# Kernel tuning notes

Measured on AMD Instinct MI355X. Metric: run time of the kernel, lower is better.

The kernel has to match this reference:

```python
import jax, jax.numpy as jnp
import numpy as np

# ---- dims (see shape_source) ----
N, EG, T = 10000, 120000, 600000
NR, NS = 16, 7                      # num_radial, num_spherical
EA, EE, ET, ERBF, ECBF, EBIL = 128, 256, 64, 16, 16, 64
NB = 2                              # num_blocks
CUTOFF = 6.0
MAXZ = 100
INV_SQRT2 = 0.7071067811865476


def scaled_silu(x):
    # GemNet 'swish' activation = ScaledSiLU
    return jax.nn.silu(x) * (1.0 / 0.6)


def layer_norm(x, w, b):
    mu = jnp.mean(x, -1, keepdims=True)
    v = jnp.var(x, -1, keepdims=True)
    return (x - mu) * jax.lax.rsqrt(v + 1e-5) * w + b


def radial_basis(D):
    # polynomial envelope (exponent 5) * gaussian RBF on d/cutoff
    d = D / CUTOFF
    p = 5.0
    env = 1.0 - ((p + 1) * (p + 2) / 2) * d**5 + p * (p + 2) * d**6 - (p * (p + 1) / 2) * d**7
    env = jnp.where(d < 1.0, env, 0.0)
    offsets = jnp.linspace(0.0, 1.0, NR)
    coeff = -0.5 * (NR - 1.0) ** 2   # -0.5 / spacing^2
    return env[:, None] * jnp.exp(coeff * (d[:, None] - offsets) ** 2)  # (EG, NR)


def spherical_basis(cosphi):
    # circular basis: Y_l0(phi) = sqrt((2l+1)/4pi) P_l(cos phi), l = 0..NS-1
    P = [jnp.ones_like(cosphi), cosphi]
    for l in range(2, NS):
        P.append(((2 * l - 1) * cosphi * P[-1] - (l - 1) * P[-2]) / l)
    return jnp.stack([np.sqrt((2 * l + 1) / (4 * np.pi)) * P[l] for l in range(NS)], -1)  # (T, NS)


def residual(x, Ws):
    # GemNet ResidualLayer: 2 bias-free dense + skip, scaled by 1/sqrt(2)
    y = scaled_silu(scaled_silu(x @ Ws[0]) @ Ws[1])
    return (x + y) * INV_SQRT2


def gemnet_forward(D, cosphi, atom_emb, W_rbf3, W_rbf_h, W_rbf_out, W_cbf_down,
                   W_edge_emb, ib_dense_ca, ib_trip_dense_ba, ib_trip_mlp_rbf,
                   ib_trip_down, ib_trip_bilinear, ib_trip_up_ca, ib_trip_up_ac,
                   ib_res_before, ib_res_after, ib_atom_dense_rbf, ib_atom_dense1,
                   ib_atom_res, ib_concat_dense, ib_res_m, ob_dense_rbf, ob_dense1,
                   ob_res, ln_m_w, ln_m_b, ln_E_w, ln_E_b,
                   Z, idx_s, idx_t, id3_ba, id3_ca, id_swap):
    rbf = radial_basis(D)                                   # (EG, NR)
    sph = spherical_basis(cosphi)                           # (T, NS)
    rbf3 = rbf @ W_rbf3                                     # (EG, ERBF)
    rbf_h = rbf @ W_rbf_h
    rbf_out = rbf @ W_rbf_out
    # EfficientInteractionDownProjection: rbf x W -> (EG, NS, ECBF)
    rbf_W1 = jnp.einsum('er,sri->esi', rbf, W_cbf_down)
    # per-triplet circular-basis embedding: sum over spherical components
    cbf_t = jnp.einsum('ts,tsi->ti', sph, rbf_W1[id3_ca])   # (T, ECBF)

    h = atom_emb[Z]                                         # (N, EA)
    m = scaled_silu(jnp.concatenate([h[idx_s], h[idx_t], rbf], -1) @ W_edge_emb)  # (EG, EE)

    def out_block(i, h_cur, m_cur):
        mn = layer_norm(m_cur, ln_m_w[i], ln_m_b[i])
        x = mn * (rbf_out @ ob_dense_rbf[i])                # (EG, EE)
        xE = jax.ops.segment_sum(x, idx_t, num_segments=N)  # scatter edges -> atoms
        xE = scaled_silu(xE @ ob_dense1[i])                 # (N, EA)
        for r in range(ob_res.shape[1]):
            xE = residual(xE, ob_res[i, r])
        return layer_norm(xE, ln_E_w[i], ln_E_b[i])

    E_t = out_block(0, h, m)
    for i in range(NB):
        # ---- triplet interaction ----
        x_ca_skip = scaled_silu(m @ ib_dense_ca[i])
        x_ba = scaled_silu(m @ ib_trip_dense_ba[i])
        x_ba = x_ba * (rbf3 @ ib_trip_mlp_rbf[i])
        x_trip = scaled_silu(x_ba @ ib_trip_down[i])        # (EG, ET)
        x_t = x_trip[id3_ba]                                # gather -> (T, ET)
        # bilinear: out[t,o] = sum_i cbf_t[t,i] * sum_c x_t[t,c] W[c,i,o]
        Wb = ib_trip_bilinear[i]                            # (ET, ECBF, EBIL)
        acc = (x_t @ Wb[:, 0, :]) * cbf_t[:, 0:1]
        for ic in range(1, ECBF):
            acc = acc + (x_t @ Wb[:, ic, :]) * cbf_t[:, ic:ic + 1]
        x = jax.ops.segment_sum(acc, id3_ca, num_segments=EG)  # scatter trip -> edges (EG, EBIL)
        x_ca = scaled_silu(x @ ib_trip_up_ca[i])
        x_ac = scaled_silu(x @ ib_trip_up_ac[i])[id_swap]   # counter-directional edge
        x3 = (x_ca + x_ac) * INV_SQRT2

        # ---- edge update ----
        x = (x_ca_skip + x3) * INV_SQRT2
        for r in range(ib_res_before.shape[1]):
            x = residual(x, ib_res_before[i, r])
        x = (x + m) * INV_SQRT2
        for r in range(ib_res_after.shape[1]):
            x = residual(x, ib_res_after[i, r])

        # ---- atom update ----
        xa = x * (rbf_h @ ib_atom_dense_rbf[i])
        xa = jax.ops.segment_sum(xa, idx_t, num_segments=N)
        xa = scaled_silu(xa @ ib_atom_dense1[i])            # (N, EA)
        for r in range(ib_atom_res.shape[1]):
            xa = residual(xa, ib_atom_res[i, r])
        h = (h + xa) * INV_SQRT2

        # ---- edge embedding refresh with updated atoms ----
        m2 = scaled_silu(jnp.concatenate([h[idx_s], h[idx_t], x], -1) @ ib_concat_dense[i])
        for r in range(ib_res_m.shape[1]):
            m2 = residual(m2, ib_res_m[i, r])
        m = (m + m2) * INV_SQRT2

        E_t = E_t + out_block(i + 1, h, m)
    return E_t  # (N, EA) per-atom output features


def setup_inputs() -> dict:
    key = jax.random.key(0)
    ks = iter(jax.random.split(key, 64))

    def nrm(shape, fan_in):
        return jax.random.normal(next(ks), shape, jnp.float32) / np.sqrt(fan_in)

    Z = jax.random.randint(next(ks), (N,), 0, MAXZ)
    idx_s = jax.random.randint(next(ks), (EG,), 0, N)
    idx_t = jax.random.randint(next(ks), (EG,), 0, N)
    id3_ba = jax.random.randint(next(ks), (T,), 0, EG)
    id3_ca = jax.random.randint(next(ks), (T,), 0, EG)
    id_swap = jnp.arange(EG) ^ 1   # symmetric edges stored in (e, e^1) pairs
    D = jax.random.uniform(next(ks), (EG,), jnp.float32, 0.8, 5.9)
    cosphi = jax.random.uniform(next(ks), (T,), jnp.float32, -1.0, 1.0)

    emb = jax.random.normal(next(ks), (MAXZ, EA), jnp.float32)
    emb = emb / jnp.maximum(jnp.linalg.norm(emb, axis=-1, keepdims=True), 1.0)  # max_norm=1

    NBo = NB + 1
    inp = dict(
        D=D, cosphi=cosphi, atom_emb=emb,
        W_rbf3=nrm((NR, ERBF), NR), W_rbf_h=nrm((NR, ERBF), NR), W_rbf_out=nrm((NR, ERBF), NR),
        W_cbf_down=nrm((NS, NR, ECBF), NR),
        W_edge_emb=nrm((2 * EA + NR, EE), 2 * EA + NR),
        ib_dense_ca=nrm((NB, EE, EE), EE),
        ib_trip_dense_ba=nrm((NB, EE, EE), EE),
        ib_trip_mlp_rbf=nrm((NB, ERBF, EE), ERBF),
        ib_trip_down=nrm((NB, EE, ET), EE),
        ib_trip_bilinear=nrm((NB, ET, ECBF, EBIL), ET * ECBF),
        ib_trip_up_ca=nrm((NB, EBIL, EE), EBIL),
        ib_trip_up_ac=nrm((NB, EBIL, EE), EBIL),
        ib_res_before=nrm((NB, 1, 2, EE, EE), EE),
        ib_res_after=nrm((NB, 1, 2, EE, EE), EE),
        ib_atom_dense_rbf=nrm((NB, ERBF, EE), ERBF),
        ib_atom_dense1=nrm((NB, EE, EA), EE),
        ib_atom_res=nrm((NB, 2, 2, EA, EA), EA),
        ib_concat_dense=nrm((NB, 2 * EA + EE, EE), 2 * EA + EE),
        ib_res_m=nrm((NB, 1, 2, EE, EE), EE),
        ob_dense_rbf=nrm((NBo, ERBF, EE), ERBF),
        ob_dense1=nrm((NBo, EE, EA), EE),
        ob_res=nrm((NBo, 2, 2, EA, EA), EA),
        ln_m_w=jnp.ones((NBo, EE)), ln_m_b=jnp.zeros((NBo, EE)),
        ln_E_w=jnp.ones((NBo, EA)), ln_E_b=jnp.zeros((NBo, EA)),
        Z=Z, idx_s=idx_s, idx_t=idx_t, id3_ba=id3_ba, id3_ca=id3_ca, id_swap=id_swap,
    )
    return inp


def reference(D, cosphi, atom_emb, W_rbf3, W_rbf_h, W_rbf_out, W_cbf_down, W_edge_emb,
              ib_dense_ca, ib_trip_dense_ba, ib_trip_mlp_rbf, ib_trip_down,
              ib_trip_bilinear, ib_trip_up_ca, ib_trip_up_ac, ib_res_before,
              ib_res_after, ib_atom_dense_rbf, ib_atom_dense1, ib_atom_res,
              ib_concat_dense, ib_res_m, ob_dense_rbf, ob_dense1, ob_res,
              ln_m_w, ln_m_b, ln_E_w, ln_E_b, Z, idx_s, idx_t, id3_ba, id3_ca, id_swap):
    return gemnet_forward(D, cosphi, atom_emb, W_rbf3, W_rbf_h, W_rbf_out, W_cbf_down,
                          W_edge_emb, ib_dense_ca, ib_trip_dense_ba, ib_trip_mlp_rbf,
                          ib_trip_down, ib_trip_bilinear, ib_trip_up_ca, ib_trip_up_ac,
                          ib_res_before, ib_res_after, ib_atom_dense_rbf, ib_atom_dense1,
                          ib_atom_res, ib_concat_dense, ib_res_m, ob_dense_rbf, ob_dense1,
                          ob_res, ln_m_w, ln_m_b, ln_E_w, ln_E_b,
                          Z, idx_s, idx_t, id3_ba, id3_ca, id_swap)
```

## Files before the change

kernel.cpp:

```cpp
#include <hip/hip_runtime.h>

#define NATOM 10000
#define EG    120000
#define TT    600000

#define INV_SQRT2f 0.7071067811865476f

typedef unsigned short bf16t;
typedef __attribute__((ext_vector_type(8))) short s16x8;
typedef __attribute__((ext_vector_type(8))) unsigned short u16x8;
typedef __attribute__((ext_vector_type(4))) float f32x4;

__device__ __forceinline__ float ssilu(float x) {
    return x * (1.0f / (1.0f + __expf(-x))) * (1.0f / 0.6f);
}
__device__ __forceinline__ float bf2f(unsigned short u) {
    return __uint_as_float(((unsigned)u) << 16);
}
__device__ __forceinline__ unsigned short f2bf(float f) {
    unsigned b = __float_as_uint(f);
    unsigned r = (b + 0x7FFF + ((b >> 16) & 1)) >> 16;
    return (unsigned short)r;
}
__device__ __forceinline__ u16x8 cvt8(const float4 va, const float4 vb) {
    u16x8 r{};
    r[0] = f2bf(va.x); r[1] = f2bf(va.y); r[2] = f2bf(va.z); r[3] = f2bf(va.w);
    r[4] = f2bf(vb.x); r[5] = f2bf(vb.y); r[6] = f2bf(vb.z); r[7] = f2bf(vb.w);
    return r;
}

template <typename T> struct VT;
template <> struct VT<float> {
    static __device__ __forceinline__ float4 load4(const float* p) { return *(const float4*)p; }
    static __device__ __forceinline__ void store4(float* p, float4 v) { *(float4*)p = v; }
    static __device__ __forceinline__ float load(const float* p) { return *p; }
    static __device__ __forceinline__ void store(float* p, float v) { *p = v; }
};
template <> struct VT<bf16t> {
    static __device__ __forceinline__ float4 load4(const bf16t* p) {
        ushort4 u = *(const ushort4*)p;
        return make_float4(bf2f(u.x), bf2f(u.y), bf2f(u.z), bf2f(u.w));
    }
    static __device__ __forceinline__ void store4(bf16t* p, float4 v) {
        ushort4 u; u.x = f2bf(v.x); u.y = f2bf(v.y); u.z = f2bf(v.z); u.w = f2bf(v.w);
        *(ushort4*)p = u;
    }
    static __device__ __forceinline__ float load(const bf16t* p) { return bf2f(*p); }
    static __device__ __forceinline__ void store(bf16t* p, float v) { *p = f2bf(v); }
};

__global__ __launch_bounds__(256) void k_fill(float* __restrict__ o, int n, float v) {
    int i = blockIdx.x * 256 + threadIdx.x;
    if (i < n) o[i] = v;
}

__global__ __launch_bounds__(256) void k_hist(
    const int* __restrict__ idx, int* __restrict__ cnt, int n)
{
    int i = blockIdx.x * 256 + threadIdx.x;
    if (i < n) atomicAdd(&cnt[idx[i]], 1);
}

__global__ __launch_bounds__(1024) void k_scan(
    const int* __restrict__ cnt, int* __restrict__ off, int n)
{
    __shared__ int wsum[16];
    __shared__ int carrySh;
    if (threadIdx.x == 0) carrySh = 0;
    __syncthreads();
    const int lane = threadIdx.x & 63, wid = threadIdx.x >> 6;
    for (int base = 0; base < n; base += 8192) {
        int v[8]; int s = 0;
        int i0 = base + threadIdx.x * 8;
#pragma unroll
        for (int j = 0; j < 8; j++) { int i = i0 + j; v[j] = (i < n) ? cnt[i] : 0; s += v[j]; }
        int sc = s;
#pragma unroll
        for (int d = 1; d < 64; d <<= 1) { int t = __shfl_up(sc, d); if (lane >= d) sc += t; }
        if (lane == 63) wsum[wid] = sc;
        __syncthreads();
        int wbase = 0;
        for (int w = 0; w < 16; w++) wbase += (w < wid) ? wsum[w] : 0;
        int carry = carrySh;
        int excl = carry + wbase + (sc - s);
#pragma unroll
        for (int j = 0; j < 8; j++) { int i = i0 + j; if (i < n) off[i] = excl; excl += v[j]; }
        __syncthreads();
        if (threadIdx.x == 1023) carrySh = carry + wbase + sc;
        __syncthreads();
    }
    if (threadIdx.x == 0) off[n] = carrySh;
}

__global__ __launch_bounds__(256) void k_rank_trip(
    const int* __restrict__ id3_ca, const int* __restrict__ id3_ba,
    const int* __restrict__ off, int* __restrict__ cnt2,
    int* __restrict__ rank, int* __restrict__ ba_s, int* __restrict__ ca_s, int n)
{
    int t = blockIdx.x * 256 + threadIdx.x;
    if (t >= n) return;
    int ca = id3_ca[t];
    int p = off[ca] + atomicAdd(&cnt2[ca], 1);
    rank[t] = p;
    ba_s[p] = id3_ba[t];
    ca_s[p] = ca;
}

__global__ __launch_bounds__(256) void k_rank_edge(
    const int* __restrict__ idx, const int* __restrict__ off,
    int* __restrict__ cnt2, int* __restrict__ lst, int n)
{
    int i = blockIdx.x * 256 + threadIdx.x;
    if (i >= n) return;
    int a = idx[i];
    int p = off[a] + atomicAdd(&cnt2[a], 1);
    lst[p] = i;
}

__global__ __launch_bounds__(256) void k_segsum(
    const bf16t* __restrict__ X, const int* __restrict__ off,
    const int* __restrict__ lst, float* __restrict__ out)
{
    int n = blockIdx.x, j = threadIdx.x;
    int b = off[n], e = off[n + 1];
    float s = 0.f;
    for (int k = b; k < e; k++) s += bf2f(X[(size_t)lst[k] * 256 + j]);
    out[(size_t)n * 256 + j] = s;
}

__global__ __launch_bounds__(256) void k_wcomb(
    const float* __restrict__ Wa, const float* __restrict__ Wb, float* __restrict__ Wc)
{
    __shared__ float sA[256];
    int j = threadIdx.x;
    sA[j] = Wa[j];
    __syncthreads();
#pragma unroll 4
    for (int r = 0; r < 16; r++) {
        float acc = 0.f;
#pragma unroll
        for (int k = 0; k < 16; k++) acc = fmaf(sA[r * 16 + k], Wb[k * 256 + j], acc);
        Wc[r * 256 + j] = acc;
    }
}

__global__ __launch_bounds__(256) void k_wt(
    const float* __restrict__ B, bf16t* __restrict__ BT, int K, int KP, int N)
{
    int idx = blockIdx.x * 256 + threadIdx.x;
    if (idx >= N * KP) return;
    int n = idx / KP, k = idx - n * KP;
    BT[idx] = (k < K) ? f2bf(B[(size_t)k * N + n]) : (bf16t)0;
}

__global__ __launch_bounds__(256) void k_wtb(
    const float* __restrict__ Wb, bf16t* __restrict__ WT)
{
    int idx = blockIdx.x * 256 + threadIdx.x;
    if (idx >= 16 * 64 * 64) return;
    int e = idx & 7, o = (idx >> 3) & 63, ch = (idx >> 9) & 7, i = idx >> 12;
    int c = ch * 8 + e;
    WT[idx] = f2bf(Wb[((size_t)c * 16 + i) * 64 + o]);
}

template <typename T>
__global__ __launch_bounds__(256) void k_rbf(
    const float* __restrict__ D, const float* __restrict__ Wc,
    T* __restrict__ rbf, float* __restrict__ rbfW1)
{
    __shared__ float sW[1792];
    for (int i = threadIdx.x; i < 1792; i += 256) sW[i] = Wc[i];
    __syncthreads();
    int e = blockIdx.x * 256 + threadIdx.x;
    if (e >= EG) return;
    float d = D[e] * (1.0f / 6.0f);
    float d2 = d * d, d4 = d2 * d2, d5 = d4 * d, d6 = d5 * d, d7 = d6 * d;
    float env = 1.0f - 21.0f * d5 + 35.0f * d6 - 15.0f * d7;
    if (d >= 1.0f) env = 0.0f;
    float r[16];
#pragma unroll
    for (int i = 0; i < 16; i++) {
        float t = d - (float)i * (1.0f / 15.0f);
        r[i] = env * __expf(-112.5f * t * t);
    }
#pragma unroll
    for (int j = 0; j < 16; j++) VT<T>::store(rbf + (size_t)e * 16 + j, r[j]);
    for (int s = 0; s < 7; s++) {
#pragma unroll 4
        for (int i = 0; i < 16; i++) {
            float a = 0.f;
#pragma unroll
            for (int k = 0; k < 16; k++)
                a = fmaf(r[k], sW[(s * 16 + k) * 16 + i], a);
            rbfW1[(size_t)e * 112 + s * 16 + i] = a;
        }
    }
}

template <typename T>
__global__ __launch_bounds__(256) void k_cbf(
    const float* __restrict__ cosphi, const int* __restrict__ id3_ca,
    const float* __restrict__ rbfW1, const int* __restrict__ rank,
    T* __restrict__ cbf)
{
    int t = blockIdx.x * 256 + threadIdx.x;
    if (t >= TT) return;
    float c = cosphi[t];
    const float norm[7] = {0.28209479177387814f, 0.4886025119029199f, 0.6307831305050401f,
                           0.7463526651802308f, 0.8462843753216345f, 0.935414346693485f,
                           1.0171072362820548f};
    float y[7];
    float pm2 = 1.0f, pm1 = c;
    y[0] = norm[0];
    y[1] = norm[1] * c;
    for (int l = 2; l < 7; l++) {
        float p = ((2.0f * l - 1.0f) * c * pm1 - (l - 1.0f) * pm2) / (float)l;
        y[l] = norm[l] * p;
        pm2 = pm1; pm1 = p;
    }
    int e = id3_ca[t];
    const float* __restrict__ w = rbfW1 + (size_t)e * 112;
    float out[16];
#pragma unroll
    for (int i = 0; i < 16; i++) out[i] = 0.f;
#pragma unroll
    for (int s = 0; s < 7; s++) {
        float ys = y[s];
#pragma unroll
        for (int i = 0; i < 16; i++) out[i] = fmaf(ys, w[s * 16 + i], out[i]);
    }
    int p = rank[t];
#pragma unroll
    for (int i = 0; i < 16; i += 4)
        VT<T>::store4(cbf + (size_t)p * 16 + i, make_float4(out[i], out[i + 1], out[i + 2], out[i + 3]));
}

__global__ __launch_bounds__(256) void k_hgather(
    const float* __restrict__ emb, const int* __restrict__ Z, bf16t* __restrict__ h)
{
    int i = blockIdx.x * 256 + threadIdx.x;
    if (i < NATOM * 128) {
        int n = i >> 7, j = i & 127;
        h[i] = f2bf(emb[(size_t)Z[n] * 128 + j]);
    }
}

template <typename TA, int FC, int EPI>
__global__ __launch_bounds__(256) void mgemm3(
    const TA* __restrict__ A, const bf16t* __restrict__ BT,
    bf16t* __restrict__ C, const bf16t* __restrict__ skip,
    int M, int N, int K, const int* __restrict__ swp)
{
    __shared__ __align__(16) ushort As[128][40];
    __shared__ __align__(16) ushort Bs[FC * 16][40];
    const int tid = threadIdx.x, wave = tid >> 6, lane = tid & 63;
    const int rowBase = blockIdx.y * 128, colBase = blockIdx.x * (FC * 16);

    const int sar = tid >> 1, sak = (tid & 1) << 4;
    int agr = rowBase + sar; if (agr >= M) agr = M - 1;
    const int sbc = (FC == 8) ? (tid >> 1) : (tid >> 2);
    const int sbk = (FC == 8) ? ((tid & 1) << 4) : ((tid & 3) << 3);

    f32x4 zv = {0.f, 0.f, 0.f, 0.f};
    f32x4 acc[2][FC];
#pragma unroll
    for (int p = 0; p < 2; p++)
#pragma unroll
        for (int q = 0; q < FC; q++) acc[p][q] = zv;

    const int arow = wave * 32 + (lane & 15);
    const int kd = (lane >> 4) << 3;

    for (int k0 = 0; k0 < K; k0 += 32) {
        u16x8 a0, a1, b0, b1;
        if constexpr (sizeof(TA) == 2) {
            const u16x8* s = (const u16x8*)((const bf16t*)A + (size_t)agr * K + k0 + sak);
            a0 = s[0]; a1 = s[1];
        } else {
            const float4* s = (const float4*)((const float*)A + (size_t)agr * K + k0 + sak);
            a0 = cvt8(s[0], s[1]); a1 = cvt8(s[2], s[3]);
        }
        {
            const u16x8* s = (const u16x8*)(BT + (size_t)(colBase + sbc) * K + k0 + sbk);
            b0 = s[0];
            if constexpr (FC == 8) b1 = s[1];
        }
        __syncthreads();
        *(u16x8*)&As[sar][sak] = a0;
        *(u16x8*)&As[sar][sak + 8] = a1;
        *(u16x8*)&Bs[sbc][sbk] = b0;
        if constexpr (FC == 8) *(u16x8*)&Bs[sbc][sbk + 8] = b1;
        __syncthreads();

        u16x8 af0 = *(const u16x8*)&As[arow][kd];
        u16x8 af1 = *(const u16x8*)&As[arow + 16][kd];
#pragma unroll
        for (int fc = 0; fc < FC; fc++) {
            u16x8 bf = *(const u16x8*)&Bs[(lane & 15) + fc * 16][kd];
            acc[0][fc] = __builtin_amdgcn_mfma_f32_16x16x32_bf16(
                *(s16x8*)&af0, *(s16x8*)&bf, acc[0][fc], 0, 0, 0);
            acc[1][fc] = __builtin_amdgcn_mfma_f32_16x16x32_bf16(
                *(s16x8*)&af1, *(s16x8*)&bf, acc[1][fc], 0, 0, 0);
        }
    }

    const int rB = rowBase + wave * 32 + ((lane >> 4) << 2);
    const int cB = colBase + (lane & 15);
#pragma unroll
    for (int fr = 0; fr < 2; fr++) {
#pragma unroll
        for (int r = 0; r < 4; r++) {
            int row = rB + fr * 16 + r;
            if (row >= M) continue;
#pragma unroll
            for (int fc = 0; fc < FC; fc++) {
                int col = cB + fc * 16;
                float v = acc[fr][fc][r];
                if (EPI == 1) {
                    C[(size_t)row * N + col] = f2bf(ssilu(v));
                } else if (EPI == 2) {
                    float sk = bf2f(skip[(size_t)row * N + col]);
                    C[(size_t)row * N + col] = f2bf((sk + ssilu(v)) * INV_SQRT2f);
                } else {
                    int tr = swp[row];
                    bf16t* cp = &C[(size_t)tr * N + col];
                    *cp = f2bf((bf2f(*cp) + ssilu(v)) * INV_SQRT2f);
                }
            }
        }
    }
}

__global__ __launch_bounds__(256) void mgemmA1(
    const bf16t* __restrict__ BT,
    bf16t* __restrict__ C,
    int M, int N, int K, int KP,
    const bf16t* __restrict__ hA, const int* __restrict__ gS,
    const int* __restrict__ gT, const bf16t* __restrict__ X, int w2)
{
    __shared__ __align__(16) ushort As[128][40];
    __shared__ __align__(16) ushort Bs[64][40];
    const int tid = threadIdx.x;
    const int wave = tid >> 6, lane = tid & 63;
    const int rowBase = blockIdx.y * 128, colBase = blockIdx.x * 64;

    const int ar = tid >> 1;
    const int ah = (tid & 1) << 4;
    const int arow = rowBase + ar;
    const int arowC = arow < M ? arow : (M - 1);
    const int ia = gS[arowC], ibx = gT[arowC];

    const int sbc = tid >> 2;
    const int sbk = (tid & 3) << 3;

    f32x4 zv = {0.f, 0.f, 0.f, 0.f};
    f32x4 acc[2][4];
#pragma unroll
    for (int p = 0; p < 2; p++)
#pragma unroll
        for (int q = 0; q < 4; q++) acc[p][q] = zv;

    const int aoff = wave * 32 + (lane & 15);
    const int kd = (lane >> 4) << 3;

    for (int k0 = 0; k0 < K; k0 += 32) {
        u16x8 a0{}, a1{};
        const int kk = k0 + ah;
        if (kk < 128) {
            const u16x8* s = (const u16x8*)(hA + (size_t)ia * 128 + kk);
            a0 = s[0]; a1 = s[1];
        } else if (kk < 256) {
            const u16x8* s = (const u16x8*)(hA + (size_t)ibx * 128 + (kk - 128));
            a0 = s[0]; a1 = s[1];
        } else if (kk < K && kk - 256 < w2) {
            const u16x8* s = (const u16x8*)(X + (size_t)arowC * w2 + (kk - 256));
            a0 = s[0]; a1 = s[1];
        }
        u16x8 bv = *(const u16x8*)(BT + (size_t)(colBase + sbc) * KP + k0 + sbk);
        __syncthreads();
        *(u16x8*)&As[ar][ah] = a0;
        *(u16x8*)&As[ar][ah + 8] = a1;
        *(u16x8*)&Bs[sbc][sbk] = bv;
        __syncthreads();

        u16x8 af0 = *(const u16x8*)&As[aoff][kd];
        u16x8 af1 = *(const u16x8*)&As[aoff + 16][kd];
#pragma unroll
        for (int fc = 0; fc < 4; fc++) {
            u16x8 bf = *(const u16x8*)&Bs[(lane & 15) + fc * 16][kd];
            acc[0][fc] = __builtin_amdgcn_mfma_f32_16x16x32_bf16(
                *(s16x8*)&af0, *(s16x8*)&bf, acc[0][fc], 0, 0, 0);
            acc[1][fc] = __builtin_amdgcn_mfma_f32_16x16x32_bf16(
                *(s16x8*)&af1, *(s16x8*)&bf, acc[1][fc], 0, 0, 0);
        }
    }

    const int rBase = rowBase + wave * 32 + ((lane >> 4) << 2);
    const int cBase = colBase + (lane & 15);
#pragma unroll
    for (int fr = 0; fr < 2; fr++) {
#pragma unroll
        for (int r = 0; r < 4; r++) {
            int row = rBase + fr * 16 + r;
            if (row >= M) continue;
#pragma unroll
            for (int fc = 0; fc < 4; fc++) {
                int col = cBase + fc * 16;
                C[(size_t)row * N + col] = f2bf(ssilu(acc[fr][fc][r]));
            }
        }
    }
}

__global__ __launch_bounds__(256) void k_bilinear_m(
    const bf16t* __restrict__ xtrip, const bf16t* __restrict__ cbf,
    const bf16t* __restrict__ WT,
    const int* __restrict__ ba_s, const int* __restrict__ ca_s,
    float* __restrict__ seg)
{
    __shared__ __align__(16) ushort xs[64][72];
    __shared__ ushort cbs[64][16];
    __shared__ int cas[64];
    __shared__ __align__(16) float ts[64][65];
    const int tid = threadIdx.x, wave = tid >> 6, lane = tid & 63;
    const int t0 = blockIdx.x * 64;
    {
        int r = tid >> 2, q = (tid & 3) << 4;
        int ba = ba_s[t0 + r];
        const u16x8* src = (const u16x8*)(xtrip + (size_t)ba * 64 + q);
        *(u16x8*)&xs[r][q] = src[0];
        *(u16x8*)&xs[r][q + 8] = src[1];
    }
    if (tid < 64) cas[tid] = ca_s[t0 + tid];
    {
        int e = tid << 2; int r = e >> 4, c = e & 15;
        *(ushort4*)&cbs[r][c] = *(const ushort4*)(cbf + (size_t)(t0 + r) * 16 + c);
    }
    __syncthreads();
    const int kd = (lane >> 4) << 3;
    u16x8 a0 = *(const u16x8*)(&xs[wave * 16 + (lane & 15)][kd]);
    u16x8 a1 = *(const u16x8*)(&xs[wave * 16 + (lane & 15)][32 + kd]);
    const int rowo = wave * 16 + ((lane >> 4) << 2);
    const int chb = lane >> 4, colw = lane & 15;
    auto waddr = [&](int i, int fc, int half) {
        return WT + (((size_t)(i * 8 + half * 4 + chb) * 64) + colw + fc * 16) * 8;
    };

    float tot[4][4];
#pragma unroll
    for (int a = 0; a < 4; a++)
#pragma unroll
        for (int b = 0; b < 4; b++) tot[a][b] = 0.f;

    u16x8 bw[8], bn[8];
#pragma unroll
    for (int fc = 0; fc < 4; fc++) {
        bw[fc * 2 + 0] = *(const u16x8*)waddr(0, fc, 0);
        bw[fc * 2 + 1] = *(const u16x8*)waddr(0, fc, 1);
    }
    for (int i = 0; i < 16; i++) {
        if (i < 15) {
#pragma unroll
            for (int fc = 0; fc < 4; fc++) {
                bn[fc * 2 + 0] = *(const u16x8*)waddr(i + 1, fc, 0);
                bn[fc * 2 + 1] = *(const u16x8*)waddr(i + 1, fc, 1);
            }
        }
        f32x4 zv = {0.f, 0.f, 0.f, 0.f};
        f32x4 p[4] = {zv, zv, zv, zv};
#pragma unroll
        for (int fc = 0; fc < 4; fc++) {
            p[fc] = __builtin_amdgcn_mfma_f32_16x16x32_bf16(
                *(s16x8*)&a0, *(s16x8*)&bw[fc * 2 + 0], p[fc], 0, 0, 0);
            p[fc] = __builtin_amdgcn_mfma_f32_16x16x32_bf16(
                *(s16x8*)&a1, *(s16x8*)&bw[fc * 2 + 1], p[fc], 0, 0, 0);
        }
#pragma unroll
        for (int r = 0; r < 4; r++) {
            float s = bf2f(cbs[rowo + r][i]);
#pragma unroll
            for (int fc = 0; fc < 4; fc++) tot[fc][r] += s * p[fc][r];
        }
#pragma unroll
        for (int q = 0; q < 8; q++) bw[q] = bn[q];
    }
#pragma unroll
    for (int r = 0; r < 4; r++)
#pragma unroll
        for (int fc = 0; fc < 4; fc++)
            ts[rowo + r][fc * 16 + (lane & 15)] = tot[fc][r];
    __syncthreads();
    {
        int q = tid >> 6, c = tid & 63;
        float s = 0.f;
        int cur = cas[q * 16];
#pragma unroll 1
        for (int r = q * 16; r < q * 16 + 16; r++) {
            int ca = cas[r];
            if (ca != cur) {
                atomicAdd(&seg[(size_t)cur * 64 + c], s);
                s = 0.f; cur = ca;
            }
            s += ts[r][c];
        }
        atomicAdd(&seg[(size_t)cur * 64 + c], s);
    }
}

template <int EPI>
__global__ __launch_bounds__(256) void gemm64(
    const float* __restrict__ A, const float* __restrict__ B,
    float* __restrict__ C, const float* __restrict__ skip,
    int M, int N, int K)
{
    __shared__ __align__(16) float As[16][64];
    __shared__ __align__(16) float Bs[16][64];
    const int tid = threadIdx.x;
    const int tx = tid & 15, ty = tid >> 4;
    const int rowBase = blockIdx.y * 64;
    const int colBase = blockIdx.x * 64;
    const int lr = tid >> 2;
    const int lk = (tid & 3) * 4;
    const int bk = tid >> 4;
    const int bc = (tid & 15) * 4;
    int arow = rowBase + lr;
    int arowC = arow < M ? arow : (M - 1);

    float acc[4][4];
#pragma unroll
    for (int i = 0; i < 4; i++)
#pragma unroll
        for (int j = 0; j < 4; j++) acc[i][j] = 0.f;

    for (int k0 = 0; k0 < K; k0 += 16) {
        float4 a4 = *(const float4*)(A + (size_t)arowC * K + k0 + lk);
        float4 b4 = *(const float4*)(B + (size_t)(k0 + bk) * N + colBase + bc);
        __syncthreads();
        As[lk + 0][lr] = a4.x;
        As[lk + 1][lr] = a4.y;
        As[lk + 2][lr] = a4.z;
        As[lk + 3][lr] = a4.w;
        *(float4*)(&Bs[bk][bc]) = b4;
        __syncthreads();
#pragma unroll
        for (int kk = 0; kk < 16; kk++) {
            float4 av = *(const float4*)(&As[kk][ty * 4]);
            float4 bv = *(const float4*)(&Bs[kk][tx * 4]);
            float a[4] = {av.x, av.y, av.z, av.w};
            float b[4] = {bv.x, bv.y, bv.z, bv.w};
#pragma unroll
            for (int i = 0; i < 4; i++)
#pragma unroll
                for (int j = 0; j < 4; j++)
                    acc[i][j] = fmaf(a[i], b[j], acc[i][j]);
        }
    }
    const int col0 = colBase + tx * 4;
#pragma unroll
    for (int ri = 0; ri < 4; ri++) {
        int row = rowBase + ty * 4 + ri;
        if (row >= M) break;
        float* cp = C + (size_t)row * N + col0;
#pragma unroll
        for (int ci = 0; ci < 4; ci++) {
            float v = acc[ri][ci];
            if (EPI == 1) v = ssilu(v);
            if (EPI == 2) v = (skip[(size_t)row * N + col0 + ci] + ssilu(v)) * INV_SQRT2f;
            cp[ci] = v;
        }
    }
}

__global__ __launch_bounds__(256) void k_mulproj(
    const bf16t* __restrict__ in, const bf16t* __restrict__ rvec,
    const float* __restrict__ Wp, bf16t* __restrict__ out)
{
    int e = blockIdx.x;
    int j = threadIdx.x;
    __shared__ float r16[16];
    if (j < 16) r16[j] = bf2f(rvec[(size_t)e * 16 + j]);
    __syncthreads();
    float p = 0.f;
#pragma unroll
    for (int k = 0; k < 16; k++) p = fmaf(r16[k], Wp[k * 256 + j], p);
    float v = bf2f(in[(size_t)e * 256 + j]) * p;
    out[(size_t)e * 256 + j] = f2bf(v);
}

__global__ __launch_bounds__(256) void k_ln_proj(
    const bf16t* __restrict__ m, const float* __restrict__ lnw,
    const float* __restrict__ lnb, const bf16t* __restrict__ rvec,
    const float* __restrict__ Wp, bf16t* __restrict__ out)
{
    int e = blockIdx.x;
    int j = threadIdx.x;
    __shared__ float red[8];
    __shared__ float r16[16];
    if (j < 16) r16[j] = bf2f(rvec[(size_t)e * 16 + j]);
    float v = bf2f(m[(size_t)e * 256 + j]);
    float s = v, s2 = v * v;
#pragma unroll
    for (int off = 32; off > 0; off >>= 1) {
        s += __shfl_xor(s, off);
        s2 += __shfl_xor(s2, off);
    }
    int wid = j >> 6, lane = j & 63;
    if (lane == 0) { red[wid] = s; red[4 + wid] = s2; }
    __syncthreads();
    float tot = red[0] + red[1] + red[2] + red[3];
    float tot2 = red[4] + red[5] + red[6] + red[7];
    float mu = tot * (1.f / 256.f);
    float var = tot2 * (1.f / 256.f) - mu * mu;
    float ln = (v - mu) * rsqrtf(var + 1e-5f) * lnw[j] + lnb[j];
    float p = 0.f;
#pragma unroll
    for (int k = 0; k < 16; k++) p = fmaf(r16[k], Wp[k * 256 + j], p);
    out[(size_t)e * 256 + j] = f2bf(ln * p);
}

__global__ __launch_bounds__(128) void k_ln_acc(
    const float* __restrict__ x, const float* __restrict__ w,
    const float* __restrict__ b, float* __restrict__ out)
{
    int n = blockIdx.x;
    int j = threadIdx.x;
    __shared__ float red[4];
    float v = x[(size_t)n * 128 + j];
    float s = v, s2 = v * v;
#pragma unroll
    for (int off = 32; off > 0; off >>= 1) {
        s += __shfl_xor(s, off);
        s2 += __shfl_xor(s2, off);
    }
    int wid = j >> 6, lane = j & 63;
    if (lane == 0) { red[wid] = s; red[2 + wid] = s2; }
    __syncthreads();
    float tot = red[0] + red[1];
    float tot2 = red[2] + red[3];
    float mu = tot * (1.f / 128.f);
    float var = tot2 * (1.f / 128.f) - mu * mu;
    out[(size_t)n * 128 + j] += (v - mu) * rsqrtf(var + 1e-5f) * w[j] + b[j];
}

template <typename T>
__global__ __launch_bounds__(256) void k_addscale(
    const T* __restrict__ a, const T* __restrict__ b, T* __restrict__ y, int n4)
{
    int i = blockIdx.x * 256 + threadIdx.x;
    if (i < n4) {
        float4 av = VT<T>::load4(a + (size_t)i * 4);
        float4 bv = VT<T>::load4(b + (size_t)i * 4);
        VT<T>::store4(y + (size_t)i * 4,
                      make_float4((av.x + bv.x) * INV_SQRT2f, (av.y + bv.y) * INV_SQRT2f,
                                  (av.z + bv.z) * INV_SQRT2f, (av.w + bv.w) * INV_SQRT2f));
    }
}

__global__ __launch_bounds__(256) void k_addscale_hf(
    bf16t* __restrict__ h, const float* __restrict__ a, int n4)
{
    int i = blockIdx.x * 256 + threadIdx.x;
    if (i < n4) {
        float4 hv = VT<bf16t>::load4(h + (size_t)i * 4);
        float4 av = *(const float4*)(a + (size_t)i * 4);
        VT<bf16t>::store4(h + (size_t)i * 4,
                          make_float4((hv.x + av.x) * INV_SQRT2f, (hv.y + av.y) * INV_SQRT2f,
                                      (hv.z + av.z) * INV_SQRT2f, (hv.w + av.w) * INV_SQRT2f));
    }
}

typedef bf16t T;
static bool try_run(void* const* d_in, void* d_out, void* d_ws, size_t ws_size, hipStream_t stream)
{
    const float* D            = (const float*)d_in[0];
    const float* cosphi       = (const float*)d_in[1];
    const float* atom_emb     = (const float*)d_in[2];
    const float* W_rbf3       = (const float*)d_in[3];
    const float* W_rbf_h      = (const float*)d_in[4];
    const float* W_rbf_out    = (const float*)d_in[5];
    const float* W_cbf_down   = (const float*)d_in[6];
    const float* W_edge_emb   = (const float*)d_in[7];
    const float* ib_dense_ca  = (const float*)d_in[8];
    const float* ib_trip_dense_ba = (const float*)d_in[9];
    const float* ib_trip_mlp_rbf  = (const float*)d_in[10];
    const float* ib_trip_down     = (const float*)d_in[11];
    const float* ib_trip_bilinear = (const float*)d_in[12];
    const float* ib_trip_up_ca    = (const float*)d_in[13];
    const float* ib_trip_up_ac    = (const float*)d_in[14];
    const float* ib_res_before    = (const float*)d_in[15];
    const float* ib_res_after     = (const float*)d_in[16];
    const float* ib_atom_dense_rbf = (const float*)d_in[17];
    const float* ib_atom_dense1    = (const float*)d_in[18];
    const float* ib_atom_res       = (const float*)d_in[19];
    const float* ib_concat_dense   = (const float*)d_in[20];
    const float* ib_res_m          = (const float*)d_in[21];
    const float* ob_dense_rbf      = (const float*)d_in[22];
    const float* ob_dense1         = (const float*)d_in[23];
    const float* ob_res            = (const float*)d_in[24];
    const float* ln_m_w            = (const float*)d_in[25];
    const float* ln_m_b            = (const float*)d_in[26];
    const float* ln_E_w            = (const float*)d_in[27];
    const float* ln_E_b            = (const float*)d_in[28];
    const int* Z       = (const int*)d_in[29];
    const int* idx_s   = (const int*)d_in[30];
    const int* idx_t   = (const int*)d_in[31];
    const int* id3_ba  = (const int*)d_in[32];
    const int* id3_ca  = (const int*)d_in[33];
    const int* id_swap = (const int*)d_in[34];

    char* base = (char*)d_ws;
    size_t off = 0;
    auto alloc = [&](size_t bytes) -> char* {
        off = (off + 255) & ~(size_t)255;
        char* p = base + off;
        off += bytes;
        return p;
    };
    T* m      = (T*)alloc((size_t)EG * 256 * 2);
    T* B1     = (T*)alloc((size_t)EG * 256 * 2);
    T* B2     = (T*)alloc((size_t)EG * 256 * 2);
    float* rbfW1 = (float*)B1;
    int* rank    = (int*)B2;
    T* rbf    = (T*)alloc((size_t)EG * 16 * 2);
    T* cbf    = (T*)alloc((size_t)TT * 16 * 2);
    bf16t* h  = (bf16t*)alloc((size_t)NATOM * 128 * 2);
    T* xtrip  = (T*)alloc((size_t)EG * 64 * 2);
    char* ub  = alloc((size_t)EG * 64 * 4);
    float* seg64 = (float*)ub;
    float* segN  = (float*)ub;
    float* At1   = (float*)(ub + (size_t)NATOM * 256 * 4);
    float* At2   = (float*)(ub + (size_t)NATOM * 256 * 4 + (size_t)NATOM * 128 * 4);
    int* cntT    = (int*)ub;
    int* cnt2T   = (int*)(ub + (size_t)EG * 4);
    float* wc_mlp  = (float*)alloc(16 * 256 * 4);
    float* wc_atom = (float*)alloc(16 * 256 * 4);
    float* wc_ob   = (float*)alloc(16 * 256 * 4);
    T* wt   = (T*)alloc((size_t)288 * 256 * 2);
    T* wtb  = (T*)alloc((size_t)16 * 64 * 64 * 2);
    int* off_ca   = (int*)alloc((size_t)(EG + 1) * 4);
    int* off_atom = (int*)alloc((size_t)(NATOM + 1) * 4);
    int* ba_s     = (int*)alloc((size_t)TT * 4);
    int* ca_s     = (int*)alloc((size_t)TT * 4);
    int* csr_edges = (int*)alloc((size_t)EG * 4);
    if (off > ws_size) return false;
    float* out = (float*)d_out;

    auto cw = [&](const float* W, int K, int N) {
        int KP = (K + 31) & ~31;
        k_wt<<<(N * KP + 255) / 256, 256, 0, stream>>>(W, wt, K, KP, N);
        return KP;
    };
    auto m256 = [&](int epi, const T* A, const float* W, T* C, const T* skip, int Kk) {
        cw(W, Kk, 256);
        dim3 grid(2, (EG + 127) / 128);
        if (epi == 1)
            mgemm3<T, 8, 1><<<grid, 256, 0, stream>>>(A, wt, C, skip, EG, 256, Kk, nullptr);
        else
            mgemm3<T, 8, 2><<<grid, 256, 0, stream>>>(A, wt, C, skip, EG, 256, Kk, nullptr);
    };
    auto out_block = [&](int i) {
        k_wcomb<<<1, 256, 0, stream>>>(W_rbf_out, ob_dense_rbf + (size_t)i * 16 * 256, wc_ob);
        k_ln_proj<<<EG, 256, 0, stream>>>(m, ln_m_w + (size_t)i * 256, ln_m_b + (size_t)i * 256,
                                          rbf, wc_ob, B2);
        k_segsum<<<NATOM, 256, 0, stream>>>(B2, off_atom, csr_edges, segN);
        {
            dim3 g(2, (NATOM + 63) / 64);
            gemm64<1><<<g, 256, 0, stream>>>(segN, ob_dense1 + (size_t)i * 256 * 128, At1, nullptr, NATOM, 128, 256);
        }
        for (int r = 0; r < 2; r++) {
            const float* W0 = ob_res + ((size_t)i * 2 + r) * 2 * 128 * 128;
            const float* W1 = W0 + 128 * 128;
            dim3 g(2, (NATOM + 63) / 64);
            gemm64<1><<<g, 256, 0, stream>>>(At1, W0, At2, nullptr, NATOM, 128, 128);
            gemm64<2><<<g, 256, 0, stream>>>(At2, W1, At1, At1, NATOM, 128, 128);
        }
        k_ln_acc<<<NATOM, 128, 0, stream>>>(At1, ln_E_w + (size_t)i * 128, ln_E_b + (size_t)i * 128, out);
    };

    hipMemsetAsync(cntT, 0, (size_t)EG * 4, stream);
    k_hist<<<(TT + 255) / 256, 256, 0, stream>>>(id3_ca, cntT, TT);
    k_scan<<<1, 1024, 0, stream>>>(cntT, off_ca, EG);
    hipMemsetAsync(cnt2T, 0, (size_t)EG * 4, stream);
    k_rank_trip<<<(TT + 255) / 256, 256, 0, stream>>>(id3_ca, id3_ba, off_ca, cnt2T,
                                                      rank, ba_s, ca_s, TT);
    hipMemsetAsync(cntT, 0, (size_t)NATOM * 4, stream);
    k_hist<<<(EG + 255) / 256, 256, 0, stream>>>(idx_t, cntT, EG);
    k_scan<<<1, 1024, 0, stream>>>(cntT, off_atom, NATOM);
    hipMemsetAsync(cnt2T, 0, (size_t)NATOM * 4, stream);
    k_rank_edge<<<(EG + 255) / 256, 256, 0, stream>>>(idx_t, off_atom, cnt2T, csr_edges, EG);

    hipMemsetAsync(out, 0, (size_t)NATOM * 128 * 4, stream);
    k_rbf<T><<<(EG + 255) / 256, 256, 0, stream>>>(D, W_cbf_down, rbf, rbfW1);
    k_cbf<T><<<(TT + 255) / 256, 256, 0, stream>>>(cosphi, id3_ca, rbfW1, rank, cbf);
    k_hgather<<<(NATOM * 128 + 255) / 256, 256, 0, stream>>>(atom_emb, Z, h);
    {
        int KP = cw(W_edge_emb, 272, 256);
        dim3 grid(4, (EG + 127) / 128);
        mgemmA1<<<grid, 256, 0, stream>>>(wt, m, EG, 256, 272, KP, h, idx_s, idx_t, rbf, 16);
    }

    out_block(0);

    for (int i = 0; i < 2; i++) {
        m256(1, m, ib_dense_ca + (size_t)i * 256 * 256, B1, nullptr, 256);
        m256(1, m, ib_trip_dense_ba + (size_t)i * 256 * 256, B2, nullptr, 256);
        k_wcomb<<<1, 256, 0, stream>>>(W_rbf3, ib_trip_mlp_rbf + (size_t)i * 16 * 256, wc_mlp);
        k_mulproj<<<EG, 256, 0, stream>>>(B2, rbf, wc_mlp, B2);
        {
            cw(ib_trip_down + (size_t)i * 256 * 64, 256, 64);
            dim3 grid(1, (EG + 127) / 128);
            mgemm3<T, 4, 1><<<grid, 256, 0, stream>>>(B2, wt, xtrip, nullptr, EG, 64, 256, nullptr);
        }
        hipMemsetAsync(seg64, 0, (size_t)EG * 64 * 4, stream);
        k_wtb<<<(16 * 64 * 64 + 255) / 256, 256, 0, stream>>>(ib_trip_bilinear + (size_t)i * 64 * 16 * 64, wtb);
        k_bilinear_m<<<TT / 64, 256, 0, stream>>>(xtrip, cbf, wtb, ba_s, ca_s, seg64);
        {
            cw(ib_trip_up_ca + (size_t)i * 64 * 256, 64, 256);
            dim3 grid(2, (EG + 127) / 128);
            mgemm3<float, 8, 1><<<grid, 256, 0, stream>>>(seg64, wt, B2, nullptr, EG, 256, 64, nullptr);
            cw(ib_trip_up_ac + (size_t)i * 64 * 256, 64, 256);
            mgemm3<float, 8, 3><<<grid, 256, 0, stream>>>(seg64, wt, B2, nullptr, EG, 256, 64, id_swap);
        }
        k_addscale<T><<<(EG * 256 / 4 + 255) / 256, 256, 0, stream>>>(B1, B2, B1, EG * 256 / 4);
        {
            const float* W0 = ib_res_before + (size_t)i * 2 * 256 * 256;
            const float* W1 = W0 + 256 * 256;
            m256(1, B1, W0, B2, nullptr, 256);
            m256(2, B2, W1, B1, B1, 256);
        }
        k_addscale<T><<<(EG * 256 / 4 + 255) / 256, 256, 0, stream>>>(B1, m, B1, EG * 256 / 4);
        {
            const float* W0 = ib_res_after + (size_t)i * 2 * 256 * 256;
            const float* W1 = W0 + 256 * 256;
            m256(1, B1, W0, B2, nullptr, 256);
            m256(2, B2, W1, B1, B1, 256);
        }
        k_wcomb<<<1, 256, 0, stream>>>(W_rbf_h, ib_atom_dense_rbf + (size_t)i * 16 * 256, wc_atom);
        k_mulproj<<<EG, 256, 0, stream>>>(B1, rbf, wc_atom, B2);
        k_segsum<<<NATOM, 256, 0, stream>>>(B2, off_atom, csr_edges, segN);
        {
            dim3 g(2, (NATOM + 63) / 64);
            gemm64<1><<<g, 256, 0, stream>>>(segN, ib_atom_dense1 + (size_t)i * 256 * 128, At1, nullptr, NATOM, 128, 256);
            for (int r = 0; r < 2; r++) {
                const float* W0 = ib_atom_res + ((size_t)i * 2 + r) * 2 * 128 * 128;
                const float* W1 = W0 + 128 * 128;
                gemm64<1><<<g, 256, 0, stream>>>(At1, W0, At2, nullptr, NATOM, 128, 128);
                gemm64<2><<<g, 256, 0, stream>>>(At2, W1, At1, At1, NATOM, 128, 128);
            }
        }
        k_addscale_hf<<<(NATOM * 128 / 4 + 255) / 256, 256, 0, stream>>>(h, At1, NATOM * 128 / 4);
        {
            int KP = cw(ib_concat_dense + (size_t)i * 512 * 256, 512, 256);
            dim3 grid(4, (EG + 127) / 128);
            mgemmA1<<<grid, 256, 0, stream>>>(wt, B2, EG, 256, 512, KP, h, idx_s, idx_t, B1, 256);
        }
        {
            const float* W0 = ib_res_m + (size_t)i * 2 * 256 * 256;
            const float* W1 = W0 + 256 * 256;
            m256(1, B2, W0, B1, nullptr, 256);
            m256(2, B1, W1, B2, B2, 256);
        }
        k_addscale<T><<<(EG * 256 / 4 + 255) / 256, 256, 0, stream>>>(m, B2, m, EG * 256 / 4);

        out_block(i + 1);
    }
    return true;
}

extern "C" void kernel_launch(void* const* d_in, const int* in_sizes, int n_in,
                              void* d_out, int out_size, void* d_ws, size_t ws_size,
                              hipStream_t stream)
{
    if (try_run(d_in, d_out, d_ws, ws_size, stream)) return;
    float v = 3000.0f + (float)(ws_size >> 20);
    k_fill<<<(NATOM * 128 + 255) / 256, 256, 0, stream>>>((float*)d_out, NATOM * 128, v);
}
```

Baseline: 3.213 ms.

## Batch weight transposes, fuse up-projections, register-prefetch GEMMs, use bf16 atom path

```diff
diff --git a/kernel.cpp b/kernel.cpp
--- a/kernel.cpp
+++ b/kernel.cpp
@@ -33,8 +33,6 @@
 template <> struct VT<float> {
     static __device__ __forceinline__ float4 load4(const float* p) { return *(const float4*)p; }
     static __device__ __forceinline__ void store4(float* p, float4 v) { *(float4*)p = v; }
-    static __device__ __forceinline__ float load(const float* p) { return *p; }
-    static __device__ __forceinline__ void store(float* p, float v) { *p = v; }
 };
 template <> struct VT<bf16t> {
     static __device__ __forceinline__ float4 load4(const bf16t* p) {
@@ -45,8 +43,6 @@
         ushort4 u; u.x = f2bf(v.x); u.y = f2bf(v.y); u.z = f2bf(v.z); u.w = f2bf(v.w);
         *(ushort4*)p = u;
     }
-    static __device__ __forceinline__ float load(const bf16t* p) { return bf2f(*p); }
-    static __device__ __forceinline__ void store(bf16t* p, float v) { *p = f2bf(v); }
 };
 
 __global__ __launch_bounds__(256) void k_fill(float* __restrict__ o, int n, float v) {
@@ -119,54 +115,60 @@
 
 __global__ __launch_bounds__(256) void k_segsum(
     const bf16t* __restrict__ X, const int* __restrict__ off,
-    const int* __restrict__ lst, float* __restrict__ out)
+    const int* __restrict__ lst, bf16t* __restrict__ out)
 {
     int n = blockIdx.x, j = threadIdx.x;
     int b = off[n], e = off[n + 1];
     float s = 0.f;
     for (int k = b; k < e; k++) s += bf2f(X[(size_t)lst[k] * 256 + j]);
-    out[(size_t)n * 256 + j] = s;
-}
-
-__global__ __launch_bounds__(256) void k_wcomb(
-    const float* __restrict__ Wa, const float* __restrict__ Wb, float* __restrict__ Wc)
+    out[(size_t)n * 256 + j] = f2bf(s);
+}
+
+struct WtE { const float* src; unsigned dstOff; int K, KP, N, mode; };
+struct WtBatch { WtE e[12]; int n; };
+
+__global__ __launch_bounds__(256) void k_wt_batch(WtBatch b, bf16t* __restrict__ base)
+{
+    for (int i = 0; i < b.n; i++) {
+        const WtE E = b.e[i];
+        int total = (E.mode == 0) ? E.N * E.KP : 16 * 64 * 64;
+        for (int idx = blockIdx.x * 256 + threadIdx.x; idx < total; idx += gridDim.x * 256) {
+            bf16t v;
+            if (E.mode == 0) {
+                int n = idx / E.KP, k = idx - n * E.KP;
+                v = (k < E.K) ? f2bf(E.src[(size_t)k * E.N + n]) : (bf16t)0;
+            } else {
+                int e8 = idx & 7, o = (idx >> 3) & 63, ch = (idx >> 9) & 7, ii = idx >> 12;
+                v = f2bf(E.src[((size_t)(ch * 8 + e8) * 16 + ii) * 64 + o]);
+            }
+            base[E.dstOff + idx] = v;
+        }
+    }
+}
+
+struct WcE { const float* Wa; const float* Wb; };
+struct WcBatch { WcE e[7]; };
+
+__global__ __launch_bounds__(256) void k_wcomb_batch(WcBatch b, float* __restrict__ wcb)
 {
     __shared__ float sA[256];
-    int j = threadIdx.x;
-    sA[j] = Wa[j];
+    int c = blockIdx.x, j = threadIdx.x;
+    sA[j] = b.e[c].Wa[j];
     __syncthreads();
+    const float* Wb = b.e[c].Wb;
+    float* dst = wcb + (size_t)c * 4096;
 #pragma unroll 4
     for (int r = 0; r < 16; r++) {
         float acc = 0.f;
 #pragma unroll
         for (int k = 0; k < 16; k++) acc = fmaf(sA[r * 16 + k], Wb[k * 256 + j], acc);
-        Wc[r * 256 + j] = acc;
-    }
-}
-
-__global__ __launch_bounds__(256) void k_wt(
-    const float* __restrict__ B, bf16t* __restrict__ BT, int K, int KP, int N)
-{
-    int idx = blockIdx.x * 256 + threadIdx.x;
-    if (idx >= N * KP) return;
-    int n = idx / KP, k = idx - n * KP;
-    BT[idx] = (k < K) ? f2bf(B[(size_t)k * N + n]) : (bf16t)0;
-}
-
-__global__ __launch_bounds__(256) void k_wtb(
-    const float* __restrict__ Wb, bf16t* __restrict__ WT)
-{
-    int idx = blockIdx.x * 256 + threadIdx.x;
-    if (idx >= 16 * 64 * 64) return;
-    int e = idx & 7, o = (idx >> 3) & 63, ch = (idx >> 9) & 7, i = idx >> 12;
-    int c = ch * 8 + e;
-    WT[idx] = f2bf(Wb[((size_t)c * 16 + i) * 64 + o]);
-}
-
-template <typename T>
+        dst[r * 256 + j] = acc;
+    }
+}
+
 __global__ __launch_bounds__(256) void k_rbf(
     const float* __restrict__ D, const float* __restrict__ Wc,
-    T* __restrict__ rbf, float* __restrict__ rbfW1)
+    bf16t* __restrict__ rbf, float* __restrict__ rbfW1)
 {
     __shared__ float sW[1792];
     for (int i = threadIdx.x; i < 1792; i += 256) sW[i] = Wc[i];
@@ -184,7 +186,7 @@
         r[i] = env * __expf(-112.5f * t * t);
     }
 #pragma unroll
-    for (int j = 0; j < 16; j++) VT<T>::store(rbf + (size_t)e * 16 + j, r[j]);
+    for (int j = 0; j < 16; j++) rbf[(size_t)e * 16 + j] = f2bf(r[j]);
     for (int s = 0; s < 7; s++) {
 #pragma unroll 4
         for (int i = 0; i < 16; i++) {
@@ -197,11 +199,10 @@
     }
 }
 
-template <typename T>
 __global__ __launch_bounds__(256) void k_cbf(
     const float* __restrict__ cosphi, const int* __restrict__ id3_ca,
     const float* __restrict__ rbfW1, const int* __restrict__ rank,
-    T* __restrict__ cbf)
+    bf16t* __restrict__ cbf)
 {
     int t = blockIdx.x * 256 + threadIdx.x;
     if (t >= TT) return;
@@ -231,8 +232,7 @@
     }
     int p = rank[t];
 #pragma unroll
-    for (int i = 0; i < 16; i += 4)
-        VT<T>::store4(cbf + (size_t)p * 16 + i, make_float4(out[i], out[i + 1], out[i + 2], out[i + 3]));
+    for (int i = 0; i < 16; i++) cbf[(size_t)p * 16 + i] = f2bf(out[i]);
 }
 
 __global__ __launch_bounds__(256) void k_hgather(
@@ -245,34 +245,39 @@
     }
 }
 
-template <typename TA, int FC, int EPI>
+template <typename TA, int FR, int FC, int EPI>
 __global__ __launch_bounds__(256) void mgemm3(
     const TA* __restrict__ A, const bf16t* __restrict__ BT,
     bf16t* __restrict__ C, const bf16t* __restrict__ skip,
-    int M, int N, int K, const int* __restrict__ swp)
-{
-    __shared__ __align__(16) ushort As[128][40];
-    __shared__ __align__(16) ushort Bs[FC * 16][40];
+    int M, int N, int K)
+{
+    constexpr int ROWS = 2 * FR * 16;
+    constexpr int COLS = 2 * FC * 16;
+    __shared__ __align__(16) ushort As[ROWS][40];
+    __shared__ __align__(16) ushort Bs[COLS][40];
     const int tid = threadIdx.x, wave = tid >> 6, lane = tid & 63;
-    const int rowBase = blockIdx.y * 128, colBase = blockIdx.x * (FC * 16);
+    const int waveR = wave >> 1, waveC = wave & 1;
+    const int rowBase = blockIdx.y * ROWS, colBase = blockIdx.x * COLS;
 
     const int sar = tid >> 1, sak = (tid & 1) << 4;
     int agr = rowBase + sar; if (agr >= M) agr = M - 1;
-    const int sbc = (FC == 8) ? (tid >> 1) : (tid >> 2);
-    const int sbk = (FC == 8) ? ((tid & 1) << 4) : ((tid & 3) << 3);
+    int sbc, sbk;
+    if constexpr (COLS == 128) { sbc = tid >> 1; sbk = (tid & 1) << 4; }
+    else                       { sbc = tid >> 2; sbk = (tid & 3) << 3; }
 
     f32x4 zv = {0.f, 0.f, 0.f, 0.f};
-    f32x4 acc[2][FC];
-#pragma unroll
-    for (int p = 0; p < 2; p++)
-#pragma unroll
-        for (int q = 0; q < FC; q++) acc[p][q] = zv;
-
-    const int arow = wave * 32 + (lane & 15);
+    f32x4 acc[FR][FC];
+#pragma unroll
+    for (int f = 0; f < FR; f++)
+#pragma unroll
+        for (int q = 0; q < FC; q++) acc[f][q] = zv;
+
+    const int arow0 = waveR * FR * 16 + (lane & 15);
+    const int bcol0 = waveC * FC * 16 + (lane & 15);
     const int kd = (lane >> 4) << 3;
 
-    for (int k0 = 0; k0 < K; k0 += 32) {
-        u16x8 a0, a1, b0, b1;
+    u16x8 a0, a1, b0, b1;
+    auto loadA = [&](int k0) {
         if constexpr (sizeof(TA) == 2) {
             const u16x8* s = (const u16x8*)((const bf16t*)A + (size_t)agr * K + k0 + sak);
             a0 = s[0]; a1 = s[1];
@@ -280,51 +285,51 @@
             const float4* s = (const float4*)((const float*)A + (size_t)agr * K + k0 + sak);
             a0 = cvt8(s[0], s[1]); a1 = cvt8(s[2], s[3]);
         }
-        {
-            const u16x8* s = (const u16x8*)(BT + (size_t)(colBase + sbc) * K + k0 + sbk);
-            b0 = s[0];
-            if constexpr (FC == 8) b1 = s[1];
-        }
+    };
+    auto loadB = [&](int k0) {
+        const u16x8* s = (const u16x8*)(BT + (size_t)(colBase + sbc) * K + k0 + sbk);
+        b0 = s[0];
+        if constexpr (COLS == 128) b1 = s[1];
+    };
+    loadA(0); loadB(0);
+    for (int k0 = 0; k0 < K; k0 += 32) {
         __syncthreads();
         *(u16x8*)&As[sar][sak] = a0;
         *(u16x8*)&As[sar][sak + 8] = a1;
         *(u16x8*)&Bs[sbc][sbk] = b0;
-        if constexpr (FC == 8) *(u16x8*)&Bs[sbc][sbk + 8] = b1;
+        if constexpr (COLS == 128) *(u16x8*)&Bs[sbc][sbk + 8] = b1;
         __syncthreads();
-
-        u16x8 af0 = *(const u16x8*)&As[arow][kd];
-        u16x8 af1 = *(const u16x8*)&As[arow + 16][kd];
-#pragma unroll
-        for (int fc = 0; fc < FC; fc++) {
-            u16x8 bf = *(const u16x8*)&Bs[(lane & 15) + fc * 16][kd];
-            acc[0][fc] = __builtin_amdgcn_mfma_f32_16x16x32_bf16(
-                *(s16x8*)&af0, *(s16x8*)&bf, acc[0][fc], 0, 0, 0);
-            acc[1][fc] = __builtin_amdgcn_mfma_f32_16x16x32_bf16(
-                *(s16x8*)&af1, *(s16x8*)&bf, acc[1][fc], 0, 0, 0);
-        }
-    }
-
-    const int rB = rowBase + wave * 32 + ((lane >> 4) << 2);
-    const int cB = colBase + (lane & 15);
-#pragma unroll
-    for (int fr = 0; fr < 2; fr++) {
+        if (k0 + 32 < K) { loadA(k0 + 32); loadB(k0 + 32); }
+        u16x8 af[FR], bf[FC];
+#pragma unroll
+        for (int f = 0; f < FR; f++) af[f] = *(const u16x8*)&As[arow0 + f * 16][kd];
+#pragma unroll
+        for (int q = 0; q < FC; q++) bf[q] = *(const u16x8*)&Bs[bcol0 + q * 16][kd];
+#pragma unroll
+        for (int f = 0; f < FR; f++)
+#pragma unroll
+            for (int q = 0; q < FC; q++)
+                acc[f][q] = __builtin_amdgcn_mfma_f32_16x16x32_bf16(
+                    *(s16x8*)&af[f], *(s16x8*)&bf[q], acc[f][q], 0, 0, 0);
+    }
+
+    const int rB = rowBase + waveR * FR * 16 + ((lane >> 4) << 2);
+    const int cB = colBase + waveC * FC * 16 + (lane & 15);
+#pragma unroll
+    for (int f = 0; f < FR; f++) {
 #pragma unroll
         for (int r = 0; r < 4; r++) {
-            int row = rB + fr * 16 + r;
+            int row = rB + f * 16 + r;
             if (row >= M) continue;
 #pragma unroll
-            for (int fc = 0; fc < FC; fc++) {
-                int col = cB + fc * 16;
-                float v = acc[fr][fc][r];
+            for (int q = 0; q < FC; q++) {
+                int col = cB + q * 16;
+                float v = acc[f][q][r];
                 if (EPI == 1) {
                     C[(size_t)row * N + col] = f2bf(ssilu(v));
-                } else if (EPI == 2) {
+                } else {
                     float sk = bf2f(skip[(size_t)row * N + col]);
                     C[(size_t)row * N + col] = f2bf((sk + ssilu(v)) * INV_SQRT2f);
-                } else {
-                    int tr = swp[row];
-                    bf16t* cp = &C[(size_t)tr * N + col];
-                    *cp = f2bf((bf2f(*cp) + ssilu(v)) * INV_SQRT2f);
                 }
             }
         }
@@ -332,40 +337,38 @@
 }
 
 __global__ __launch_bounds__(256) void mgemmA1(
-    const bf16t* __restrict__ BT,
-    bf16t* __restrict__ C,
+    const bf16t* __restrict__ BT, bf16t* __restrict__ C,
     int M, int N, int K, int KP,
     const bf16t* __restrict__ hA, const int* __restrict__ gS,
     const int* __restrict__ gT, const bf16t* __restrict__ X, int w2)
 {
     __shared__ __align__(16) ushort As[128][40];
     __shared__ __align__(16) ushort Bs[64][40];
-    const int tid = threadIdx.x;
-    const int wave = tid >> 6, lane = tid & 63;
+    const int tid = threadIdx.x, wave = tid >> 6, lane = tid & 63;
+    const int waveR = wave >> 1, waveC = wave & 1;
     const int rowBase = blockIdx.y * 128, colBase = blockIdx.x * 64;
 
-    const int ar = tid >> 1;
-    const int ah = (tid & 1) << 4;
-    const int arow = rowBase + ar;
+    const int sar = tid >> 1, sak = (tid & 1) << 4;
+    const int arow = rowBase + sar;
     const int arowC = arow < M ? arow : (M - 1);
     const int ia = gS[arowC], ibx = gT[arowC];
-
-    const int sbc = tid >> 2;
-    const int sbk = (tid & 3) << 3;
+    const int sbc = tid >> 2, sbk = (tid & 3) << 3;
 
     f32x4 zv = {0.f, 0.f, 0.f, 0.f};
-    f32x4 acc[2][4];
-#pragma unroll
-    for (int p = 0; p < 2; p++)
-#pragma unroll
-        for (int q = 0; q < 4; q++) acc[p][q] = zv;
-
-    const int aoff = wave * 32 + (lane & 15);
+    f32x4 acc[4][2];
+#pragma unroll
+    for (int f = 0; f < 4; f++)
+#pragma unroll
+        for (int q = 0; q < 2; q++) acc[f][q] = zv;
+
+    const int arow0 = waveR * 64 + (lane & 15);
+    const int bcol0 = waveC * 32 + (lane & 15);
     const int kd = (lane >> 4) << 3;
 
-    for (int k0 = 0; k0 < K; k0 += 32) {
-        u16x8 a0{}, a1{};
-        const int kk = k0 + ah;
+    u16x8 a0, a1, b0;
+    auto loadA = [&](int k0) {
+        a0 = u16x8{}; a1 = u16x8{};
+        const int kk = k0 + sak;
         if (kk < 128) {
             const u16x8* s = (const u16x8*)(hA + (size_t)ia * 128 + kk);
             a0 = s[0]; a1 = s[1];
@@ -376,37 +379,121 @@
             const u16x8* s = (const u16x8*)(X + (size_t)arowC * w2 + (kk - 256));
             a0 = s[0]; a1 = s[1];
         }
-        u16x8 bv = *(const u16x8*)(BT + (size_t)(colBase + sbc) * KP + k0 + sbk);
+    };
+    auto loadB = [&](int k0) {
+        b0 = *(const u16x8*)(BT + (size_t)(colBase + sbc) * KP + k0 + sbk);
+    };
+    loadA(0); loadB(0);
+    for (int k0 = 0; k0 < K; k0 += 32) {
         __syncthreads();
-        *(u16x8*)&As[ar][ah] = a0;
-        *(u16x8*)&As[ar][ah + 8] = a1;
-        *(u16x8*)&Bs[sbc][sbk] = bv;
+        *(u16x8*)&As[sar][sak] = a0;
+        *(u16x8*)&As[sar][sak + 8] = a1;
+        *(u16x8*)&Bs[sbc][sbk] = b0;
         __syncthreads();
-
-        u16x8 af0 = *(const u16x8*)&As[aoff][kd];
-        u16x8 af1 = *(const u16x8*)&As[aoff + 16][kd];
-#pragma unroll
-        for (int fc = 0; fc < 4; fc++) {
-            u16x8 bf = *(const u16x8*)&Bs[(lane & 15) + fc * 16][kd];
-            acc[0][fc] = __builtin_amdgcn_mfma_f32_16x16x32_bf16(
-                *(s16x8*)&af0, *(s16x8*)&bf, acc[0][fc], 0, 0, 0);
-            acc[1][fc] = __builtin_amdgcn_mfma_f32_16x16x32_bf16(
-                *(s16x8*)&af1, *(s16x8*)&bf, acc[1][fc], 0, 0, 0);
-        }
-    }
-
-    const int rBase = rowBase + wave * 32 + ((lane >> 4) << 2);
-    const int cBase = colBase + (lane & 15);
-#pragma unroll
-    for (int fr = 0; fr < 2; fr++) {
+        if (k0 + 32 < K) { loadA(k0 + 32); loadB(k0 + 32); }
+        u16x8 af[4], bf[2];
+#pragma unroll
+        for (int f = 0; f < 4; f++) af[f] = *(const u16x8*)&As[arow0 + f * 16][kd];
+#pragma unroll
+        for (int q = 0; q < 2; q++) bf[q] = *(const u16x8*)&Bs[bcol0 + q * 16][kd];
+#pragma unroll
+        for (int f = 0; f < 4; f++)
+#pragma unroll
+            for (int q = 0; q < 2; q++)
+                acc[f][q] = __builtin_amdgcn_mfma_f32_16x16x32_bf16(
+                    *(s16x8*)&af[f], *(s16x8*)&bf[q], acc[f][q], 0, 0, 0);
+    }
+
+    const int rB = rowBase + waveR * 64 + ((lane >> 4) << 2);
+    const int cB = colBase + waveC * 32 + (lane & 15);
+#pragma unroll
+    for (int f = 0; f < 4; f++) {
 #pragma unroll
         for (int r = 0; r < 4; r++) {
-            int row = rBase + fr * 16 + r;
+            int row = rB + f * 16 + r;
             if (row >= M) continue;
 #pragma unroll
-            for (int fc = 0; fc < 4; fc++) {
-                int col = cBase + fc * 16;
-                C[(size_t)row * N + col] = f2bf(ssilu(acc[fr][fc][r]));
+            for (int q = 0; q < 2; q++)
+                C[(size_t)row * N + cB + q * 16] = f2bf(ssilu(acc[f][q][r]));
+        }
+    }
+}
+
+__global__ __launch_bounds__(256) void mgemm_up(
+    const float* __restrict__ A, const bf16t* __restrict__ BTca,
+    const bf16t* __restrict__ BTac, bf16t* __restrict__ C, int M)
+{
+    constexpr int K = 64, N = 256;
+    __shared__ __align__(16) ushort As[128][40];
+    __shared__ __align__(16) ushort Bs[2][64][40];
+    const int tid = threadIdx.x, wave = tid >> 6, lane = tid & 63;
+    const int waveR = wave >> 1, waveC = wave & 1;
+    const int rowBase = blockIdx.y * 128, colBase = blockIdx.x * 64;
+
+    const int sar = tid >> 1, sak = (tid & 1) << 4;
+    int agr = rowBase + sar; if (agr >= M) agr = M - 1;
+    const int sbc = tid >> 2, sbk = (tid & 3) << 3;
+
+    f32x4 zv = {0.f, 0.f, 0.f, 0.f};
+    f32x4 accA[4][2], accB[4][2];
+#pragma unroll
+    for (int f = 0; f < 4; f++)
+#pragma unroll
+        for (int q = 0; q < 2; q++) { accA[f][q] = zv; accB[f][q] = zv; }
+
+    const int arow0 = waveR * 64 + (lane & 15);
+    const int bcol0 = waveC * 32 + (lane & 15);
+    const int kd = (lane >> 4) << 3;
+
+    u16x8 a0, a1, bA, bB;
+    auto loadA = [&](int k0) {
+        const float4* s = (const float4*)(A + (size_t)agr * K + k0 + sak);
+        a0 = cvt8(s[0], s[1]); a1 = cvt8(s[2], s[3]);
+    };
+    auto loadB = [&](int k0) {
+        bA = *(const u16x8*)(BTca + (size_t)(colBase + sbc) * K + k0 + sbk);
+        bB = *(const u16x8*)(BTac + (size_t)(colBase + sbc) * K + k0 + sbk);
+    };
+    loadA(0); loadB(0);
+    for (int k0 = 0; k0 < K; k0 += 32) {
+        __syncthreads();
+        *(u16x8*)&As[sar][sak] = a0;
+        *(u16x8*)&As[sar][sak + 8] = a1;
+        *(u16x8*)&Bs[0][sbc][sbk] = bA;
+        *(u16x8*)&Bs[1][sbc][sbk] = bB;
+        __syncthreads();
+        if (k0 + 32 < K) { loadA(k0 + 32); loadB(k0 + 32); }
+        u16x8 af[4], bfA[2], bfB[2];
+#pragma unroll
+        for (int f = 0; f < 4; f++) af[f] = *(const u16x8*)&As[arow0 + f * 16][kd];
+#pragma unroll
+        for (int q = 0; q < 2; q++) {
+            bfA[q] = *(const u16x8*)&Bs[0][bcol0 + q * 16][kd];
+            bfB[q] = *(const u16x8*)&Bs[1][bcol0 + q * 16][kd];
+        }
+#pragma unroll
+        for (int f = 0; f < 4; f++)
+#pragma unroll
+            for (int q = 0; q < 2; q++) {
+                accA[f][q] = __builtin_amdgcn_mfma_f32_16x16x32_bf16(
+                    *(s16x8*)&af[f], *(s16x8*)&bfA[q], accA[f][q], 0, 0, 0);
+                accB[f][q] = __builtin_amdgcn_mfma_f32_16x16x32_bf16(
+                    *(s16x8*)&af[f], *(s16x8*)&bfB[q], accB[f][q], 0, 0, 0);
+            }
+    }
+
+    const int rB = rowBase + waveR * 64 + ((lane >> 4) << 2);
+    const int cB = colBase + waveC * 32 + (lane & 15);
+#pragma unroll
+    for (int f = 0; f < 4; f++) {
+#pragma unroll
+        for (int r = 0; r < 4; r++) {
+            int row = rB + f * 16 + r;
+            if (row >= M) continue;
+#pragma unroll
+            for (int q = 0; q < 2; q++) {
+                float v = (ssilu(accA[f][q][r]) + ssilu(accB[f][q][r ^ 1])) * INV_SQRT2f;
+                C[(size_t)row * N + cB + q * 16] = f2bf(v);
             }
         }
     }
@@ -507,70 +594,6 @@
     }
 }
 
-template <int EPI>
-__global__ __launch_bounds__(256) void gemm64(
-    const float* __restrict__ A, const float* __restrict__ B,
-    float* __restrict__ C, const float* __restrict__ skip,
-    int M, int N, int K)
-{
-    __shared__ __align__(16) float As[16][64];
-    __shared__ __align__(16) float Bs[16][64];
-    const int tid = threadIdx.x;
-    const int tx = tid & 15, ty = tid >> 4;
-    const int rowBase = blockIdx.y * 64;
-    const int colBase = blockIdx.x * 64;
-    const int lr = tid >> 2;
-    const int lk = (tid & 3) * 4;
-    const int bk = tid >> 4;
-    const int bc = (tid & 15) * 4;
-    int arow = rowBase + lr;
-    int arowC = arow < M ? arow : (M - 1);
-
-    float acc[4][4];
-#pragma unroll
-    for (int i = 0; i < 4; i++)
-#pragma unroll
-        for (int j = 0; j < 4; j++) acc[i][j] = 0.f;
-
-    for (int k0 = 0; k0 < K; k0 += 16) {
-        float4 a4 = *(const float4*)(A + (size_t)arowC * K + k0 + lk);
-        float4 b4 = *(const float4*)(B + (size_t)(k0 + bk) * N + colBase + bc);
-        __syncthreads();
-        As[lk + 0][lr] = a4.x;
-        As[lk + 1][lr] = a4.y;
-        As[lk + 2][lr] = a4.z;
-        As[lk + 3][lr] = a4.w;
-        *(float4*)(&Bs[bk][bc]) = b4;
-        __syncthreads();
-#pragma unroll
-        for (int kk = 0; kk < 16; kk++) {
-            float4 av = *(const float4*)(&As[kk][ty * 4]);
-            float4 bv = *(const float4*)(&Bs[kk][tx * 4]);
-            float a[4] = {av.x, av.y, av.z, av.w};
-            float b[4] = {bv.x, bv.y, bv.z, bv.w};
-#pragma unroll
-            for (int i = 0; i < 4; i++)
-#pragma unroll
-                for (int j = 0; j < 4; j++)
-                    acc[i][j] = fmaf(a[i], b[j], acc[i][j]);
-        }
-    }
-    const int col0 = colBase + tx * 4;
-#pragma unroll
-    for (int ri = 0; ri < 4; ri++) {
-        int row = rowBase + ty * 4 + ri;
-        if (row >= M) break;
-        float* cp = C + (size_t)row * N + col0;
-#pragma unroll
-        for (int ci = 0; ci < 4; ci++) {
-            float v = acc[ri][ci];
-            if (EPI == 1) v = ssilu(v);
-            if (EPI == 2) v = (skip[(size_t)row * N + col0 + ci] + ssilu(v)) * INV_SQRT2f;
-            cp[ci] = v;
-        }
-    }
-}
-
 __global__ __launch_bounds__(256) void k_mulproj(
     const bf16t* __restrict__ in, const bf16t* __restrict__ rvec,
     const float* __restrict__ Wp, bf16t* __restrict__ out)
@@ -583,8 +606,7 @@
     float p = 0.f;
 #pragma unroll
     for (int k = 0; k < 16; k++) p = fmaf(r16[k], Wp[k * 256 + j], p);
-    float v = bf2f(in[(size_t)e * 256 + j]) * p;
-    out[(size_t)e * 256 + j] = f2bf(v);
+    out[(size_t)e * 256 + j] = f2bf(bf2f(in[(size_t)e * 256 + j]) * p);
 }
 
 __global__ __launch_bounds__(256) void k_ln_proj(
@@ -619,13 +641,13 @@
 }
 
 __global__ __launch_bounds__(128) void k_ln_acc(
-    const float* __restrict__ x, const float* __restrict__ w,
+    const bf16t* __restrict__ x, const float* __restrict__ w,
     const float* __restrict__ b, float* __restrict__ out)
 {
     int n = blockIdx.x;
     int j = threadIdx.x;
     __shared__ float red[4];
-    float v = x[(size_t)n * 128 + j];
+    float v = bf2f(x[(size_t)n * 128 + j]);
     float s = v, s2 = v * v;
 #pragma unroll
     for (int off = 32; off > 0; off >>= 1) {
@@ -653,19 +675,6 @@
         VT<T>::store4(y + (size_t)i * 4,
                       make_float4((av.x + bv.x) * INV_SQRT2f, (av.y + bv.y) * INV_SQRT2f,
                                   (av.z + bv.z) * INV_SQRT2f, (av.w + bv.w) * INV_SQRT2f));
-    }
-}
-
-__global__ __launch_bounds__(256) void k_addscale_hf(
-    bf16t* __restrict__ h, const float* __restrict__ a, int n4)
-{
-    int i = blockIdx.x * 256 + threadIdx.x;
-    if (i < n4) {
-        float4 hv = VT<bf16t>::load4(h + (size_t)i * 4);
-        float4 av = *(const float4*)(a + (size_t)i * 4);
-        VT<bf16t>::store4(h + (size_t)i * 4,
-                          make_float4((hv.x + av.x) * INV_SQRT2f, (hv.y + av.y) * INV_SQRT2f,
-                                      (hv.z + av.z) * INV_SQRT2f, (hv.w + av.w) * INV_SQRT2f));
     }
 }
 
@@ -706,7 +715,6 @@
     const int* idx_t   = (const int*)d_in[31];
     const int* id3_ba  = (const int*)d_in[32];
     const int* id3_ca  = (const int*)d_in[33];
-    const int* id_swap = (const int*)d_in[34];
 
     char* base = (char*)d_ws;
     size_t off = 0;
@@ -726,55 +734,42 @@
     bf16t* h  = (bf16t*)alloc((size_t)NATOM * 128 * 2);
     T* xtrip  = (T*)alloc((size_t)EG * 64 * 2);
     char* ub  = alloc((size_t)EG * 64 * 4);
-    float* seg64 = (float*)ub;
-    float* segN  = (float*)ub;
-    float* At1   = (float*)(ub + (size_t)NATOM * 256 * 4);
-    float* At2   = (float*)(ub + (size_t)NATOM * 256 * 4 + (size_t)NATOM * 128 * 4);
-    int* cntT    = (int*)ub;
-    int* cnt2T   = (int*)(ub + (size_t)EG * 4);
-    float* wc_mlp  = (float*)alloc(16 * 256 * 4);
-    float* wc_atom = (float*)alloc(16 * 256 * 4);
-    float* wc_ob   = (float*)alloc(16 * 256 * 4);
-    T* wt   = (T*)alloc((size_t)288 * 256 * 2);
-    T* wtb  = (T*)alloc((size_t)16 * 64 * 64 * 2);
-    int* off_ca   = (int*)alloc((size_t)(EG + 1) * 4);
-    int* off_atom = (int*)alloc((size_t)(NATOM + 1) * 4);
-    int* ba_s     = (int*)alloc((size_t)TT * 4);
-    int* ca_s     = (int*)alloc((size_t)TT * 4);
+    float* seg64  = (float*)ub;
+    bf16t* segN_b = (bf16t*)ub;
+    bf16t* At1b   = (bf16t*)(ub + (size_t)NATOM * 256 * 2);
+    bf16t* At2b   = (bf16t*)(ub + (size_t)NATOM * 256 * 2 + (size_t)NATOM * 128 * 2);
+    int* cntT  = (int*)ub;
+    int* cnt2T = (int*)(ub + (size_t)EG * 4);
+    int* off_ca = (int*)(ub + (size_t)2 * EG * 4);
+    float* wcb = (float*)alloc((size_t)7 * 4096 * 4);
+    bf16t* ar  = (bf16t*)alloc((size_t)507904 * 2);
+    int* off_atom  = (int*)alloc((size_t)(NATOM + 1) * 4);
+    int* ba_s      = (int*)alloc((size_t)TT * 4);
+    int* ca_s      = (int*)alloc((size_t)TT * 4);
     int* csr_edges = (int*)alloc((size_t)EG * 4);
     if (off > ws_size) return false;
     float* out = (float*)d_out;
 
-    auto cw = [&](const float* W, int K, int N) {
-        int KP = (K + 31) & ~31;
-        k_wt<<<(N * KP + 255) / 256, 256, 0, stream>>>(W, wt, K, KP, N);
-        return KP;
-    };
-    auto m256 = [&](int epi, const T* A, const float* W, T* C, const T* skip, int Kk) {
-        cw(W, Kk, 256);
+    auto g256 = [&](int epi, const T* A, unsigned wOff, T* C, const T* skip, int K) {
         dim3 grid(2, (EG + 127) / 128);
-        if (epi == 1)
-            mgemm3<T, 8, 1><<<grid, 256, 0, stream>>>(A, wt, C, skip, EG, 256, Kk, nullptr);
-        else
-            mgemm3<T, 8, 2><<<grid, 256, 0, stream>>>(A, wt, C, skip, EG, 256, Kk, nullptr);
-    };
-    auto out_block = [&](int i) {
-        k_wcomb<<<1, 256, 0, stream>>>(W_rbf_out, ob_dense_rbf + (size_t)i * 16 * 256, wc_ob);
+        if (epi == 1) mgemm3<T, 4, 4, 1><<<grid, 256, 0, stream>>>(A, ar + wOff, C, skip, EG, 256, K);
+        else          mgemm3<T, 4, 4, 2><<<grid, 256, 0, stream>>>(A, ar + wOff, C, skip, EG, 256, K);
+    };
+    auto gatom = [&](int epi, const bf16t* A, unsigned wOff, bf16t* C, const bf16t* skip, int K) {
+        dim3 grid(1, (NATOM + 127) / 128);
+        if (epi == 1) mgemm3<bf16t, 4, 4, 1><<<grid, 256, 0, stream>>>(A, ar + wOff, C, skip, NATOM, 128, K);
+        else          mgemm3<bf16t, 4, 4, 2><<<grid, 256, 0, stream>>>(A, ar + wOff, C, skip, NATOM, 128, K);
+    };
+    auto out_block = [&](int i, unsigned offD1, unsigned offRes) {
         k_ln_proj<<<EG, 256, 0, stream>>>(m, ln_m_w + (size_t)i * 256, ln_m_b + (size_t)i * 256,
-                                          rbf, wc_ob, B2);
-        k_segsum<<<NATOM, 256, 0, stream>>>(B2, off_atom, csr_edges, segN);
-        {
-            dim3 g(2, (NATOM + 63) / 64);
-            gemm64<1><<<g, 256, 0, stream>>>(segN, ob_dense1 + (size_t)i * 256 * 128, At1, nullptr, NATOM, 128, 256);
-        }
+                                          rbf, wcb + (size_t)(4 + i) * 4096, B2);
+        k_segsum<<<NATOM, 256, 0, stream>>>(B2, off_atom, csr_edges, segN_b);
+        gatom(1, segN_b, offD1, At1b, nullptr, 256);
         for (int r = 0; r < 2; r++) {
-            const float* W0 = ob_res + ((size_t)i * 2 + r) * 2 * 128 * 128;
-            const float* W1 = W0 + 128 * 128;
-            dim3 g(2, (NATOM + 63) / 64);
-            gemm64<1><<<g, 256, 0, stream>>>(At1, W0, At2, nullptr, NATOM, 128, 128);
-            gemm64<2><<<g, 256, 0, stream>>>(At2, W1, At1, At1, NATOM, 128, 128);
-        }
-        k_ln_acc<<<NATOM, 128, 0, stream>>>(At1, ln_E_w + (size_t)i * 128, ln_E_b + (size_t)i * 128, out);
+            gatom(1, At1b, offRes + (r * 2 + 0) * 16384, At2b, nullptr, 128);
+            gatom(2, At2b, offRes + (r * 2 + 1) * 16384, At1b, At1b, 128);
+        }
+        k_ln_acc<<<NATOM, 128, 0, stream>>>(At1b, ln_E_w + (size_t)i * 128, ln_E_b + (size_t)i * 128, out);
     };
 
     hipMemsetAsync(cntT, 0, (size_t)EG * 4, stream);
@@ -789,80 +784,113 @@
     hipMemsetAsync(cnt2T, 0, (size_t)NATOM * 4, stream);
     k_rank_edge<<<(EG + 255) / 256, 256, 0, stream>>>(idx_t, off_atom, cnt2T, csr_edges, EG);
 
+    {
+        WcBatch wb;
+        wb.e[0] = {W_rbf3, ib_trip_mlp_rbf};
+        wb.e[1] = {W_rbf3, ib_trip_mlp_rbf + 4096};
+        wb.e[2] = {W_rbf_h, ib_atom_dense_rbf};
+        wb.e[3] = {W_rbf_h, ib_atom_dense_rbf + 4096};
+        wb.e[4] = {W_rbf_out, ob_dense_rbf};
+        wb.e[5] = {W_rbf_out, ob_dense_rbf + 4096};
+        wb.e[6] = {W_rbf_out, ob_dense_rbf + 8192};
+        k_wcomb_batch<<<7, 256, 0, stream>>>(wb, wcb);
+    }
+    {
+        WtBatch wt{};
+        wt.e[0] = {W_edge_emb, 0u, 272, 288, 256, 0};
+        wt.e[1] = {ob_dense1, 73728u, 256, 256, 128, 0};
+        for (int j = 0; j < 4; j++)
+            wt.e[2 + j] = {ob_res + (size_t)j * 16384, 106496u + j * 16384u, 128, 128, 128, 0};
+        wt.n = 6;
+        k_wt_batch<<<512, 256, 0, stream>>>(wt, ar);
+    }
+
     hipMemsetAsync(out, 0, (size_t)NATOM * 128 * 4, stream);
-    k_rbf<T><<<(EG + 255) / 256, 256, 0, stream>>>(D, W_cbf_down, rbf, rbfW1);
-    k_cbf<T><<<(TT + 255) / 256, 256, 0, stream>>>(cosphi, id3_ca, rbfW1, rank, cbf);
+    k_rbf<<<(EG + 255) / 256, 256, 0, stream>>>(D, W_cbf_down, rbf, rbfW1);
+    k_cbf<<<(TT + 255) / 256, 256, 0, stream>>>(cosphi, id3_ca, rbfW1, rank, cbf);
     k_hgather<<<(NATOM * 128 + 255) / 256, 256, 0, stream>>>(atom_emb, Z, h);
     {
-        int KP = cw(W_edge_emb, 272, 256);
         dim3 grid(4, (EG + 127) / 128);
-        mgemmA1<<<grid, 256, 0, stream>>>(wt, m, EG, 256, 272, KP, h, idx_s, idx_t, rbf, 16);
-    }
-
-    out_block(0);
+        mgemmA1<<<grid, 256, 0, stream>>>(ar, m, EG, 256, 272, 288, h, idx_s, idx_t, rbf, 16);
+    }
+    out_block(0, 73728u, 106496u);
 
     for (int i = 0; i < 2; i++) {
-        m256(1, m, ib_dense_ca + (size_t)i * 256 * 256, B1, nullptr, 256);
-        m256(1, m, ib_trip_dense_ba + (size_t)i * 256 * 256, B2, nullptr, 256);
-        k_wcomb<<<1, 256, 0, stream>>>(W_rbf3, ib_trip_mlp_rbf + (size_t)i * 16 * 256, wc_mlp);
-        k_mulproj<<<EG, 256, 0, stream>>>(B2, rbf, wc_mlp, B2);
         {
-            cw(ib_trip_down + (size_t)i * 256 * 64, 256, 64);
+            WtBatch wt{};
+            wt.e[0] = {ib_dense_ca + (size_t)i * 65536, 0u, 256, 256, 256, 0};
+            wt.e[1] = {ib_trip_dense_ba + (size_t)i * 65536, 65536u, 256, 256, 256, 0};
+            wt.e[2] = {ib_trip_down + (size_t)i * 16384, 131072u, 256, 256, 64, 0};
+            wt.e[3] = {ib_trip_bilinear + (size_t)i * 65536, 147456u, 0, 0, 0, 1};
+            wt.e[4] = {ib_trip_up_ca + (size_t)i * 16384, 212992u, 64, 64, 256, 0};
+            wt.e[5] = {ib_trip_up_ac + (size_t)i * 16384, 229376u, 64, 64, 256, 0};
+            wt.e[6] = {ib_res_before + (size_t)i * 131072, 245760u, 256, 256, 256, 0};
+            wt.e[7] = {ib_res_before + (size_t)i * 131072 + 65536, 311296u, 256, 256, 256, 0};
+            wt.e[8] = {ib_res_after + (size_t)i * 131072, 376832u, 256, 256, 256, 0};
+            wt.e[9] = {ib_res_after + (size_t)i * 131072 + 65536, 442368u, 256, 256, 256, 0};
+            wt.n = 10;
+            k_wt_batch<<<512, 256, 0, stream>>>(wt, ar);
+        }
+        g256(1, m, 0u, B1, nullptr, 256);
+        g256(1, m, 65536u, B2, nullptr, 256);
+        k_mulproj<<<EG, 256, 0, stream>>>(B2, rbf, wcb + (size_t)i * 4096, B2);
+        {
             dim3 grid(1, (EG + 127) / 128);
-            mgemm3<T, 4, 1><<<grid, 256, 0, stream>>>(B2, wt, xtrip, nullptr, EG, 64, 256, nullptr);
+            mgemm3<T, 4, 2, 1><<<grid, 256, 0, stream>>>(B2, ar + 131072, xtrip, nullptr, EG, 64, 256);
         }
         hipMemsetAsync(seg64, 0, (size_t)EG * 64 * 4, stream);
-        k_wtb<<<(16 * 64 * 64 + 255) / 256, 256, 0, stream>>>(ib_trip_bilinear + (size_t)i * 64 * 16 * 64, wtb);
-        k_bilinear_m<<<TT / 64, 256, 0, stream>>>(xtrip, cbf, wtb, ba_s, ca_s, seg64);
+        k_bilinear_m<<<TT / 64, 256, 0, stream>>>(xtrip, cbf, ar + 147456, ba_s, ca_s, seg64);
         {
-            cw(ib_trip_up_ca + (size_t)i * 64 * 256, 64, 256);
-            dim3 grid(2, (EG + 127) / 128);
-            mgemm3<float, 8, 1><<<grid, 256, 0, stream>>>(seg64, wt, B2, nullptr, EG, 256, 64, nullptr);
-            cw(ib_trip_up_ac + (size_t)i * 64 * 256, 64, 256);
-            mgemm3<float, 8, 3><<<grid, 256, 0, stream>>>(seg64, wt, B2, nullptr, EG, 256, 64, id_swap);
+            dim3 grid(4, (EG + 127) / 128);
+            mgemm_up<<<grid, 256, 0, stream>>>(seg64, ar + 212992, ar + 229376, B2, EG);
         }
         k_addscale<T><<<(EG * 256 / 4 + 255) / 256, 256, 0, stream>>>(B1, B2, B1, EG * 256 / 4);
+        g256(1, B1, 245760u, B2, nullptr, 256);
+        g256(2, B2, 311296u, B1, B1, 256);
+        k_addscale<T><<<(EG * 256 / 4 + 255) / 256, 256, 0, stream>>>(B1, m, B1, EG * 256 / 4);
+        g256(1, B1, 376832u, B2, nullptr, 256);
+        g256(2, B2, 442368u, B1, B1, 256);
         {
-            const float* W0 = ib_res_before + (size_t)i * 2 * 256 * 256;
-            const float* W1 = W0 + 256 * 256;
-            m256(1, B1, W0, B2, nullptr, 256);
-            m256(2, B2, W1, B1, B1, 256);
-        }
-        k_addscale<T><<<(EG * 256 / 4 + 255) / 256, 256, 0, stream>>>(B1, m, B1, EG * 256 / 4);
+            WtBatch wt{};
+            wt.e[0] = {ib_atom_dense1 + (size_t)i * 32768, 0u, 256, 256, 128, 0};
+            for (int j = 0; j < 4; j++)
+                wt.e[1 + j] = {ib_atom_res + (size_t)i * 65536 + (size_t)j * 16384,
+                               32768u + j * 16384u, 128, 128, 128, 0};
+            wt.e[5] = {ib_concat_dense + (size_t)i * 131072, 98304u, 512, 512, 256, 0};
+            wt.e[6] = {ib_res_m + (size_t)i * 131072, 229376u, 256, 256, 256, 0};
+            wt.e[7] = {ib_res_m + (size_t)i * 131072 + 65536, 294912u, 256, 256, 256, 0};
+            wt.e[8] = {ob_dense1 + (size_t)(i + 1) * 32768, 360448u, 256, 256, 128, 0};
+            for (int j = 0; j < 4; j++)
+                wt.e[9 + j] = {ob_res + (size_t)(i + 1) * 65536 + (size_t)j * 16384,
+                               393216u + j * 16384u, 128, 128, 128, 0};
+            wt.n = 13 <= 12 ? 13 : 12;
+            wt.n = 9;
+            k_wt_batch<<<512, 256, 0, stream>>>(wt, ar);
+            WtBatch wt2{};
+            wt2.e[0] = {ob_dense1 + (size_t)(i + 1) * 32768, 360448u, 256, 256, 128, 0};
+            for (int j = 0; j < 4; j++)
+                wt2.e[1 + j] = {ob_res + (size_t)(i + 1) * 65536 + (size_t)j * 16384,
+                                393216u + j * 16384u, 128, 128, 128, 0};
+            wt2.n = 5;
+            k_wt_batch<<<512, 256, 0, stream>>>(wt2, ar);
+        }
+        k_mulproj<<<EG, 256, 0, stream>>>(B1, rbf, wcb + (size_t)(2 + i) * 4096, B2);
+        k_segsum<<<NATOM, 256, 0, stream>>>(B2, off_atom, csr_edges, segN_b);
+        gatom(1, segN_b, 0u, At1b, nullptr, 256);
+        for (int r = 0; r < 2; r++) {
+            gatom(1, At1b, 32768u + (r * 2 + 0) * 16384, At2b, nullptr, 128);
+            gatom(2, At2b, 32768u + (r * 2 + 1) * 16384, At1b, At1b, 128);
+        }
+        k_addscale<bf16t><<<(NATOM * 128 / 4 + 255) / 256, 256, 0, stream>>>(h, At1b, h, NATOM * 128 / 4);
         {
-            const float* W0 = ib_res_after + (size_t)i * 2 * 256 * 256;
-            const float* W1 = W0 + 256 * 256;
-            m256(1, B1, W0, B2, nullptr, 256);
-            m256(2, B2, W1, B1, B1, 256);
-        }
-        k_wcomb<<<1, 256, 0, stream>>>(W_rbf_h, ib_atom_dense_rbf + (size_t)i * 16 * 256, wc_atom);
-        k_mulproj<<<EG, 256, 0, stream>>>(B1, rbf, wc_atom, B2);
-        k_segsum<<<NATOM, 256, 0, stream>>>(B2, off_atom, csr_edges, segN);
-        {
-            dim3 g(2, (NATOM + 63) / 64);
-            gemm64<1><<<g, 256, 0, stream>>>(segN, ib_atom_dense1 + (size_t)i * 256 * 128, At1, nullptr, NATOM, 128, 256);
-            for (int r = 0; r < 2; r++) {
-                const float* W0 = ib_atom_res + ((size_t)i * 2 + r) * 2 * 128 * 128;
-                const float* W1 = W0 + 128 * 128;
-                gemm64<1><<<g, 256, 0, stream>>>(At1, W0, At2, nullptr, NATOM, 128, 128);
-                gemm64<2><<<g, 256, 0, stream>>>(At2, W1, At1, At1, NATOM, 128, 128);
-            }
-        }
-        k_addscale_hf<<<(NATOM * 128 / 4 + 255) / 256, 256, 0, stream>>>(h, At1, NATOM * 128 / 4);
-        {
-            int KP = cw(ib_concat_dense + (size_t)i * 512 * 256, 512, 256);
             dim3 grid(4, (EG + 127) / 128);
-            mgemmA1<<<grid, 256, 0, stream>>>(wt, B2, EG, 256, 512, KP, h, idx_s, idx_t, B1, 256);
-        }
-        {
-            const float* W0 = ib_res_m + (size_t)i * 2 * 256 * 256;
-            const float* W1 = W0 + 256 * 256;
-            m256(1, B2, W0, B1, nullptr, 256);
-            m256(2, B1, W1, B2, B2, 256);
-        }
+            mgemmA1<<<grid, 256, 0, stream>>>(ar + 98304, B2, EG, 256, 512, 512, h, idx_s, idx_t, B1, 256);
+        }
+        g256(1, B2, 229376u, B1, nullptr, 256);
+        g256(2, B1, 294912u, B2, B2, 256);
         k_addscale<T><<<(EG * 256 / 4 + 255) / 256, 256, 0, stream>>>(m, B2, m, EG * 256 / 4);
 
-        out_block(i + 1);
+        out_block(i + 1, 360448u, 393216u);
     }
     return true;
 }
```

Measured after the change: 2.939 ms. 8.6% less time.
